# Optimization experiments

Hardware: AMD Instinct MI355X
Metric: run time of the kernel (lower is better)

Reference implementation:

```python
import jax, jax.numpy as jnp
import numpy as np

B, K, S, H, V, T = 32, 5, 64, 768, 30522, 40
SEP = 102


def setup_inputs() -> dict:
    key = jax.random.key(0)
    ks = jax.random.split(key, 8)
    s = 0.02
    return {
        "src": jax.random.normal(ks[0], (B, S, H), jnp.float32),
        "E": jax.random.normal(ks[1], (V, H), jnp.float32) * s,
        "Wa": jax.random.normal(ks[2], (H, H), jnp.float32) * s,
        "Ua": jax.random.normal(ks[3], (H, H), jnp.float32) * s,
        "va": jax.random.normal(ks[4], (H,), jnp.float32) * s,
        "W_ih": jax.random.normal(ks[5], (3 * H, 2 * H), jnp.float32) * s,
        "W_hh": jax.random.normal(ks[6], (3 * H, H), jnp.float32) * s,
        "b_ih": jnp.zeros((3 * H,), jnp.float32),
        "b_hh": jnp.zeros((3 * H,), jnp.float32),
        "Wo": jax.random.normal(ks[7], (V, H), jnp.float32) * s,
        "bo": jnp.zeros((V,), jnp.float32),
    }


def _decoder(tok, src, h, E, Wa, Ua, va, W_ih, W_hh, b_ih, b_hh, Wo, bo):
    # tok [N] int, src [N,S,H], h [N,H] -> (logits [N,V], h_new [N,H])
    emb = E[tok]                                              # [N,H]
    e = jnp.tanh(src @ Wa + (h @ Ua)[:, None, :]) @ va        # [N,S]
    a = jax.nn.softmax(e, axis=-1)
    ctx = jnp.einsum('ns,nsd->nd', a, src)                    # [N,H]
    x = jnp.concatenate([emb, ctx], axis=-1)                  # [N,2H]
    gx = x @ W_ih.T + b_ih
    gh = h @ W_hh.T + b_hh
    xr, xz, xn = jnp.split(gx, 3, axis=-1)
    hr, hz, hn = jnp.split(gh, 3, axis=-1)
    r = jax.nn.sigmoid(xr + hr)
    z = jax.nn.sigmoid(xz + hz)
    n = jnp.tanh(xn + r * hn)
    h2 = (1.0 - z) * n + z * h
    return h2 @ Wo.T + bo, h2


def _search(src, E, Wa, Ua, va, W_ih, W_hh, b_ih, b_hh, Wo, bo):
    P = (E, Wa, Ua, va, W_ih, W_hh, b_ih, b_hh, Wo, bo)
    # step 0: start token 102, zero hidden
    tok0 = jnp.full((B,), SEP, jnp.int32)
    logits, h = _decoder(tok0, src, jnp.zeros((B, H), src.dtype), *P)
    logp = jax.nn.log_softmax(logits, axis=-1)
    scores, toks = jax.lax.top_k(logp, K)                     # [B,K]
    hiddens = jnp.broadcast_to(h[:, None, :], (B, K, H))
    src_k = jnp.broadcast_to(src[:, None], (B, K, S, H)).reshape(B * K, S, H)
    no_prob = jnp.full((V,), -1e9, src.dtype).at[SEP].set(0.0)
    beam_mask = jnp.arange(K) < K - 1  # original normalizes only first k-1 segments

    def body(carry, _):
        toks, maps, hiddens, scores, ended, lengths = carry
        # parent hidden per beam (gather by backpointer), decode all beams at once
        h_in = jnp.take_along_axis(hiddens, maps[:, :, None], axis=1)  # [B,K,H]
        logits, h_new = _decoder(toks.reshape(-1), src_k, h_in.reshape(B * K, H), *P)
        logp = jax.nn.log_softmax(logits, axis=-1).reshape(B, K, V)
        logp = jnp.where(ended[:, :, None] == 0, logp, no_prob)
        lengths = lengths + (ended == 0).astype(lengths.dtype)
        cand = logp + scores[:, :, None]                      # [B,K,V]
        denom = jnp.where(beam_mask, lengths ** 0.7, 1.0)     # [B,K]
        norm = (cand / denom[:, :, None]).reshape(B, K * V)
        _, idx = jax.lax.top_k(norm, K)                       # [B,K]
        new_scores = jnp.take_along_axis(cand.reshape(B, K * V), idx, axis=1)
        new_toks = (idx % V).astype(jnp.int32)
        new_maps = (idx // V).astype(jnp.int32)
        ended = jnp.where(new_toks == SEP, 1.0, ended)
        new_carry = (new_toks, new_maps, h_new.reshape(B, K, H), new_scores, ended, lengths)
        return new_carry, (new_toks, new_maps)

    carry0 = (toks.astype(jnp.int32), jnp.zeros((B, K), jnp.int32), hiddens,
              scores, jnp.zeros((B, K), src.dtype), jnp.zeros((B, K), src.dtype))
    carryF, (toks_seq, maps_seq) = jax.lax.scan(body, carry0, None, length=T - 1)
    toks_all = jnp.concatenate([toks[None].astype(jnp.int32), toks_seq], axis=0)   # [T,B,K]
    maps_all = jnp.concatenate([jnp.zeros((1, B, K), jnp.int32), maps_seq], axis=0)
    final_scores = carryF[3]
    best = jnp.argmax(final_scores, axis=1).astype(jnp.int32)  # [B]

    def back(idx, tm):
        tk, mp = tm
        out = jnp.take_along_axis(tk, idx[:, None], axis=1)[:, 0]
        nxt = jnp.take_along_axis(mp, idx[:, None], axis=1)[:, 0]
        return nxt, out

    _, outs = jax.lax.scan(back, best, (toks_all, maps_all), reverse=True)
    return outs.T, final_scores  # tokens [B,T], scores [B,K]


def reference(src, E, Wa, Ua, va, W_ih, W_hh, b_ih, b_hh, Wo, bo):
    tokens, _ = _search(src, E, Wa, Ua, va, W_ih, W_hh, b_ih, b_hh, Wo, bo)
    return tokens
```

## Files before the change

kernel.cpp:

```cpp
#include <hip/hip_runtime.h>
#include <hip/hip_cooperative_groups.h>
#include <cmath>

namespace cg = cooperative_groups;

#define Hdim 768
#define Bb 32
#define Kb 5
#define Ss 64
#define Vv 30522
#define Tt 40
#define SEPTOK 102
#define NTLOG 477

typedef __attribute__((ext_vector_type(2))) float f32x2;
typedef __attribute__((ext_vector_type(4))) float f32x4;

struct Params {
    const float *src, *E, *Wa, *Ua, *va, *W_ih, *W_hh, *b_ih, *b_hh, *Wo, *bo;
    float *srcWa, *hA, *hB, *h_tmp, *h_g, *hUa, *xbuf, *gxE, *gx, *gh, *logits;
    float *mt_g; double *st_g; float *t5v; int *t5j;
    float *mx, *lgs, *scores, *ended, *lengths;
    int *toks_cur, *maps_cur, *toks_all, *maps_all, *outTok;
};

__device__ __forceinline__ bool betterf(float va, int ja, float vb, int jb) {
    return (va > vb) || (va == vb && ja < jb);
}
__device__ __forceinline__ void ins5(float* tv, int* tj, float v, int j) {
    if (!betterf(v, j, tv[4], tj[4])) return;
    tv[4] = v; tj[4] = j;
#pragma unroll
    for (int q = 4; q > 0; q--) {
        if (betterf(tv[q], tj[q], tv[q - 1], tj[q - 1])) {
            float t = tv[q]; tv[q] = tv[q - 1]; tv[q - 1] = t;
            int  ti = tj[q]; tj[q] = tj[q - 1]; tj[q - 1] = ti;
        }
    }
}
__device__ __forceinline__ void ins5p(float* tv, int* tj, float* tx,
                                      float v, int j, float x) {
    if (!betterf(v, j, tv[4], tj[4])) return;
    tv[4] = v; tj[4] = j; tx[4] = x;
#pragma unroll
    for (int q = 4; q > 0; q--) {
        if (betterf(tv[q], tj[q], tv[q - 1], tj[q - 1])) {
            float t = tv[q]; tv[q] = tv[q - 1]; tv[q - 1] = t;
            int  ti = tj[q]; tj[q] = tj[q - 1]; tj[q - 1] = ti;
            float tz = tx[q]; tx[q] = tx[q - 1]; tx[q - 1] = tz;
        }
    }
}

union SMem {
    struct { float xs[32][162]; float wt[32][68]; } g;
    struct { float hu[Hdim]; float va[Hdim]; float e[Ss]; float a[Ss];
             float ctx[Hdim]; float gx[2304]; } at;
    struct { float sc[Kb], den[Kb], end[Kb], len[Kb], mxs[Kb], lgv[Kb];
             float mv[256 * 5]; int mj[256 * 5]; float mxp[256 * 5];
             float rv[512]; int rj[512]; float rx[512]; double rd[512];
             int selj[Kb]; float selx[Kb]; } tk;
};

__device__ void gemm512(SMem& sm, const Params& P, int t, int N, int xsrc,
    int i0, int Pdim, const float* __restrict__ W, int ldW, bool pmaj,
    const float* __restrict__ bias, float* __restrict__ outp, int ldO, int Icap)
{
    const int tid = threadIdx.x;
    const int ty = tid >> 5, tx = tid & 31;
    const float* h_old = (t & 1) ? P.hB : P.hA;

    float acc[10][2];
#pragma unroll
    for (int j = 0; j < 10; j++) { acc[j][0] = 0.f; acc[j][1] = 0.f; }

    for (int c0 = 0; c0 < Pdim; c0 += 32) {
        __syncthreads();
        for (int e = tid; e < 160 * 32; e += 512) {
            int r = e >> 5, p = e & 31;
            int n = (r < N) ? r : (N - 1);
            float v = 0.f;
            if (xsrc == 0) {
                if (t != 0) {
                    int par = (n / Kb) * Kb + P.maps_cur[n];
                    v = h_old[(size_t)par * Hdim + c0 + p];
                }
            } else {
                int tok = (t == 0) ? SEPTOK : P.toks_cur[n];
                v = P.E[(size_t)tok * Hdim + c0 + p];
            }
            sm.g.xs[p][r] = v;
        }
        if (pmaj) {
            int p = tid >> 4, i4 = (tid & 15) * 4;
            int gi = i0 + i4;
            f32x4 a;
            if (gi + 3 < Icap) {
                a = *(const f32x4*)&W[(size_t)(c0 + p) * ldW + gi];
            } else {
#pragma unroll
                for (int u = 0; u < 4; u++) {
                    int g = gi + u; if (g >= Icap) g = Icap - 1;
                    a[u] = W[(size_t)(c0 + p) * ldW + g];
                }
            }
            *(f32x4*)&sm.g.wt[p][i4] = a;
        } else {
            int c = tid >> 3, p4 = (tid & 7) * 4;
            int gi = i0 + c; if (gi >= Icap) gi = Icap - 1;
            f32x4 a = *(const f32x4*)&W[(size_t)gi * ldW + c0 + p4];
            sm.g.wt[p4 + 0][c] = a[0]; sm.g.wt[p4 + 1][c] = a[1];
            sm.g.wt[p4 + 2][c] = a[2]; sm.g.wt[p4 + 3][c] = a[3];
        }
        __syncthreads();
        float part[10][2];
#pragma unroll
        for (int j = 0; j < 10; j++) { part[j][0] = 0.f; part[j][1] = 0.f; }
#pragma unroll
        for (int p = 0; p < 32; p++) {
            f32x2 w2 = *(const f32x2*)&sm.g.wt[p][tx * 2];
            float xr[10];
#pragma unroll
            for (int j = 0; j < 10; j += 2) {
                f32x2 xv = *(const f32x2*)&sm.g.xs[p][ty * 10 + j];
                xr[j] = xv.x; xr[j + 1] = xv.y;
            }
#pragma unroll
            for (int j = 0; j < 10; j++) {
                part[j][0] = fmaf(xr[j], w2.x, part[j][0]);
                part[j][1] = fmaf(xr[j], w2.y, part[j][1]);
            }
        }
#pragma unroll
        for (int j = 0; j < 10; j++) {
            acc[j][0] = __fadd_rn(acc[j][0], part[j][0]);
            acc[j][1] = __fadd_rn(acc[j][1], part[j][1]);
        }
    }
#pragma unroll
    for (int j = 0; j < 10; j++) {
        int r = ty * 10 + j;
        if (r < N) {
#pragma unroll
            for (int u = 0; u < 2; u++) {
                int gi = i0 + tx * 2 + u;
                if (gi < Icap) {
                    float v = acc[j][u];
                    if (bias) v = __fadd_rn(v, bias[gi]);
                    outp[(size_t)r * ldO + gi] = v;
                }
            }
        }
    }
}

__device__ void logits_tile(SMem& sm, const Params& P, int t, int N, int task)
{
    const int tid = threadIdx.x;
    const int ty = tid >> 5, tx = tid & 31;
    const int i0 = task * 64;
    const float* h_new = (t & 1) ? P.hA : P.hB;
    const int rowMul = (t == 0) ? Kb : 1;

    float acc[10][2];
#pragma unroll
    for (int j = 0; j < 10; j++) { acc[j][0] = 0.f; acc[j][1] = 0.f; }

    for (int c0 = 0; c0 < Hdim; c0 += 32) {
        __syncthreads();
        for (int e = tid; e < 160 * 32; e += 512) {
            int r = e >> 5, p = e & 31;
            int n = (r < N) ? r : (N - 1);
            sm.g.xs[p][r] = h_new[((size_t)n * rowMul) * Hdim + c0 + p];
        }
        {
            int c = tid >> 3, p4 = (tid & 7) * 4;
            int gi = i0 + c; if (gi >= Vv) gi = Vv - 1;
            f32x4 a = *(const f32x4*)&P.Wo[(size_t)gi * Hdim + c0 + p4];
            sm.g.wt[p4 + 0][c] = a[0]; sm.g.wt[p4 + 1][c] = a[1];
            sm.g.wt[p4 + 2][c] = a[2]; sm.g.wt[p4 + 3][c] = a[3];
        }
        __syncthreads();
        float part[10][2];
#pragma unroll
        for (int j = 0; j < 10; j++) { part[j][0] = 0.f; part[j][1] = 0.f; }
#pragma unroll
        for (int p = 0; p < 32; p++) {
            f32x2 w2 = *(const f32x2*)&sm.g.wt[p][tx * 2];
            float xr[10];
#pragma unroll
            for (int j = 0; j < 10; j += 2) {
                f32x2 xv = *(const f32x2*)&sm.g.xs[p][ty * 10 + j];
                xr[j] = xv.x; xr[j + 1] = xv.y;
            }
#pragma unroll
            for (int j = 0; j < 10; j++) {
                part[j][0] = fmaf(xr[j], w2.x, part[j][0]);
                part[j][1] = fmaf(xr[j], w2.y, part[j][1]);
            }
        }
#pragma unroll
        for (int j = 0; j < 10; j++) {
            acc[j][0] = __fadd_rn(acc[j][0], part[j][0]);
            acc[j][1] = __fadd_rn(acc[j][1], part[j][1]);
        }
    }
#pragma unroll
    for (int j = 0; j < 10; j++) {
        int r = ty * 10 + j;
        int g0 = i0 + tx * 2, g1 = g0 + 1;
        float x0 = (g0 < Vv) ? __fadd_rn(acc[j][0], P.bo[g0]) : -INFINITY;
        float x1 = (g1 < Vv) ? __fadd_rn(acc[j][1], P.bo[g1]) : -INFINITY;
        float mr = fmaxf(x0, x1);
#pragma unroll
        for (int off = 16; off; off >>= 1)
            mr = fmaxf(mr, __shfl_xor(mr, off, 32));
        double s = (double)expf(__fsub_rn(x0, mr)) + (double)expf(__fsub_rn(x1, mr));
#pragma unroll
        for (int off = 16; off; off >>= 1)
            s += __shfl_xor(s, off, 32);
        float tv[5]; int tj[5];
#pragma unroll
        for (int q = 0; q < 5; q++) { tv[q] = -INFINITY; tj[q] = 0x7fffffff; }
        ins5(tv, tj, x0, (g0 < Vv) ? g0 : 0x7fffffff);
        ins5(tv, tj, x1, (g1 < Vv) ? g1 : 0x7fffffff);
#pragma unroll
        for (int lv = 1; lv < 32; lv <<= 1) {
            float pv[5]; int pj[5];
#pragma unroll
            for (int q = 0; q < 5; q++) {
                pv[q] = __shfl_xor(tv[q], lv, 32);
                pj[q] = __shfl_xor(tj[q], lv, 32);
            }
#pragma unroll
            for (int q = 0; q < 5; q++) ins5(tv, tj, pv[q], pj[q]);
        }
        if (tx == 0 && r < N) {
            P.mt_g[(size_t)task * 160 + r] = mr;
            P.st_g[(size_t)task * 160 + r] = s;
#pragma unroll
            for (int q = 0; q < 5; q++) {
                P.t5v[((size_t)task * 160 + r) * 5 + q] = tv[q];
                P.t5j[((size_t)task * 160 + r) * 5 + q] = tj[q];
            }
        }
    }
}

__global__ __launch_bounds__(512) void step_k(Params P)
{
    cg::grid_group grid = cg::this_grid();
    __shared__ SMem sm;
    const int tid = threadIdx.x;
    const int gdim = gridDim.x;

    for (int t = 0; t < Tt; t++) {
        const int N = (t == 0) ? Bb : Bb * Kb;
        const int Kcur = (t == 0) ? 1 : Kb;
        float* h_new = (t & 1) ? P.hA : P.hB;
        const float* h_old = (t & 1) ? P.hB : P.hA;

        for (int task = blockIdx.x; task < 84; task += gdim) {
            if (task < 12)
                gemm512(sm, P, t, N, 0, task * 64, Hdim, P.Ua, Hdim, true,
                        nullptr, P.hUa, Hdim, Hdim);
            else if (task < 48)
                gemm512(sm, P, t, N, 0, (task - 12) * 64, Hdim, P.W_hh, Hdim, false,
                        P.b_hh, P.gh, 2304, 2304);
            else
                gemm512(sm, P, t, N, 1, (task - 48) * 64, Hdim, P.W_ih, 1536, false,
                        nullptr, P.gxE, 2304, 2304);
        }
        grid.sync();

        for (int n = blockIdx.x; n < N; n += gdim) {
            int b = n / Kcur;
            for (int j = tid; j < Hdim; j += 512) {
                sm.at.hu[j] = P.hUa[(size_t)n * Hdim + j];
                sm.at.va[j] = P.va[j];
            }
            __syncthreads();
            {
                int wv = tid >> 6, ln = tid & 63;
                for (int s = wv * 8; s < wv * 8 + 8; s++) {
                    const float* sw = P.srcWa + (size_t)(b * Ss + s) * Hdim;
                    double p = 0.0;
                    for (int j = ln; j < Hdim; j += 64) {
                        float tv = tanhf(__fadd_rn(sw[j], sm.at.hu[j]));
                        p = ::fma((double)tv, (double)sm.at.va[j], p);
                    }
                    for (int off = 32; off; off >>= 1) p += __shfl_down(p, off, 64);
                    if (ln == 0) sm.at.e[s] = (float)p;
                }
            }
            __syncthreads();
            if (tid < 64) {
                float v = sm.at.e[tid], m = v;
                for (int off = 32; off; off >>= 1) m = fmaxf(m, __shfl_xor(m, off, 64));
                float p = expf(__fsub_rn(v, m));
                double sum = (double)p;
                for (int off = 32; off; off >>= 1) sum += __shfl_xor(sum, off, 64);
                sm.at.a[tid] = __fdiv_rn(p, (float)sum);
            }
            __syncthreads();
            for (int j = tid; j < Hdim; j += 512) {
                double acc = 0.0;
                for (int s = 0; s < Ss; s++)
                    acc = ::fma((double)sm.at.a[s],
                                (double)P.src[(size_t)(b * Ss + s) * Hdim + j], acc);
                sm.at.ctx[j] = (float)acc;
            }
            __syncthreads();
            for (int i = tid; i < 2304; i += 512) {
                const float* wr = P.W_ih + (size_t)i * 1536 + 768;
                float accv = 0.f, part = 0.f;
                for (int p = 0; p < 768; p += 4) {
                    f32x4 w4 = *(const f32x4*)&wr[p];
                    part = fmaf(sm.at.ctx[p + 0], w4[0], part);
                    part = fmaf(sm.at.ctx[p + 1], w4[1], part);
                    part = fmaf(sm.at.ctx[p + 2], w4[2], part);
                    part = fmaf(sm.at.ctx[p + 3], w4[3], part);
                    if ((p & 31) == 28) { accv = __fadd_rn(accv, part); part = 0.f; }
                }
                sm.at.gx[i] = __fadd_rn(__fadd_rn(P.gxE[(size_t)n * 2304 + i], accv),
                                        P.b_ih[i]);
            }
            __syncthreads();
            int par = 0;
            if (t != 0) par = (n / Kb) * Kb + P.maps_cur[n];
            for (int i = tid; i < Hdim; i += 512) {
                float xr = sm.at.gx[i], xz = sm.at.gx[768 + i], xn = sm.at.gx[1536 + i];
                const float* ghr = P.gh + (size_t)n * 2304;
                float hr = ghr[i], hz = ghr[768 + i], hn = ghr[1536 + i];
                float r  = __fdiv_rn(1.f, __fadd_rn(1.f, expf(-__fadd_rn(xr, hr))));
                float z  = __fdiv_rn(1.f, __fadd_rn(1.f, expf(-__fadd_rn(xz, hz))));
                float nn = tanhf(__fadd_rn(xn, __fmul_rn(r, hn)));
                float hv = (t == 0) ? 0.f : h_old[(size_t)par * Hdim + i];
                float h2 = __fadd_rn(__fmul_rn(__fsub_rn(1.f, z), nn), __fmul_rn(z, hv));
                if (t == 0) {
                    for (int k = 0; k < Kb; k++)
                        h_new[(size_t)(n * Kb + k) * Hdim + i] = h2;
                } else {
                    h_new[(size_t)n * Hdim + i] = h2;
                }
            }
            __syncthreads();
        }
        grid.sync();

        for (int task = blockIdx.x; task < NTLOG; task += gdim)
            logits_tile(sm, P, t, N, task);
        grid.sync();

        for (int b = blockIdx.x; b < Bb; b += gdim) {
            if (tid < Kb) {
                if (t == 0) {
                    sm.tk.sc[tid] = 0.f; sm.tk.end[tid] = 0.f; sm.tk.len[tid] = 0.f;
                    sm.tk.den[tid] = 1.f;
                } else {
                    float e0 = P.ended[b * Kb + tid];
                    float ln = __fadd_rn(P.lengths[b * Kb + tid], (e0 == 0.f) ? 1.f : 0.f);
                    sm.tk.sc[tid]  = P.scores[b * Kb + tid];
                    sm.tk.end[tid] = e0;
                    sm.tk.len[tid] = ln;
                    sm.tk.den[tid] = (tid < Kb - 1) ? (float)pow((double)ln, (double)0.7f) : 1.f;
                }
            }
            __syncthreads();
            for (int k = 0; k < Kcur; k++) {
                bool active = (t == 0) || (sm.tk.end[k] == 0.f);
                if (!active) {
                    if (tid == 0) { sm.tk.mxs[k] = 0.f; sm.tk.lgv[k] = 0.f; }
                    __syncthreads();
                    continue;
                }
                int n = b * Kcur + k;
                float m = -INFINITY;
                for (int tile = tid; tile < NTLOG; tile += 512)
                    m = fmaxf(m, P.mt_g[(size_t)tile * 160 + n]);
                sm.tk.rv[tid] = m; __syncthreads();
                for (int off = 256; off; off >>= 1) {
                    if (tid < off) sm.tk.rv[tid] = fmaxf(sm.tk.rv[tid], sm.tk.rv[tid + off]);
                    __syncthreads();
                }
                m = sm.tk.rv[0];
                double s = 0.0;
                for (int tile = tid; tile < NTLOG; tile += 512)
                    s += P.st_g[(size_t)tile * 160 + n] *
                         exp((double)(P.mt_g[(size_t)tile * 160 + n] - m));
                __syncthreads();
                sm.tk.rd[tid] = s; __syncthreads();
                for (int off = 256; off; off >>= 1) {
                    if (tid < off) sm.tk.rd[tid] += sm.tk.rd[tid + off];
                    __syncthreads();
                }
                if (tid == 0) {
                    sm.tk.mxs[k] = m;
                    float sf = (float)sm.tk.rd[0];
                    sm.tk.lgv[k] = (float)log((double)sf);
                }
                __syncthreads();
            }
            float tv[5]; int tj[5]; float txx[5];
#pragma unroll
            for (int q = 0; q < 5; q++) { tv[q] = -INFINITY; tj[q] = 0x7fffffff; txx[q] = 0.f; }
            if (tid < 256) {
                int tot = Kcur * NTLOG * 5;
                for (int c = tid; c < tot; c += 256) {
                    int k = c / (NTLOG * 5);
                    if (t != 0 && sm.tk.end[k] != 0.f) continue;
                    int rm = c - k * NTLOG * 5;
                    int tile = rm / 5, q = rm - tile * 5;
                    int n = b * Kcur + k;
                    int gi = P.t5j[((size_t)tile * 160 + n) * 5 + q];
                    if (gi == 0x7fffffff) continue;
                    float x = P.t5v[((size_t)tile * 160 + n) * 5 + q];
                    float lp  = __fsub_rn(__fsub_rn(x, sm.tk.mxs[k]), sm.tk.lgv[k]);
                    float val = __fdiv_rn(__fadd_rn(lp, sm.tk.sc[k]), sm.tk.den[k]);
                    ins5p(tv, tj, txx, val, k * Vv + gi, x);
                }
            }
            if (tid == 0 && t != 0) {
                for (int k = 0; k < Kcur; k++)
                    if (sm.tk.end[k] != 0.f) {
                        float val = __fdiv_rn(sm.tk.sc[k], sm.tk.den[k]);
                        ins5p(tv, tj, txx, val, k * Vv + SEPTOK, 0.f);
                    }
            }
            if (tid < 256) {
#pragma unroll
                for (int q = 0; q < 5; q++) {
                    sm.tk.mv[tid * 5 + q] = tv[q];
                    sm.tk.mj[tid * 5 + q] = tj[q];
                    sm.tk.mxp[tid * 5 + q] = txx[q];
                }
            }
            __syncthreads();
            for (int pass = 0; pass < Kb; pass++) {
                if (tid < 256) {
                    float bv = -INFINITY; int bj = 0x7fffffff; float bx = 0.f;
#pragma unroll
                    for (int q = 0; q < 5; q++) {
                        float v = sm.tk.mv[tid * 5 + q]; int j = sm.tk.mj[tid * 5 + q];
                        if (betterf(v, j, bv, bj)) { bv = v; bj = j; bx = sm.tk.mxp[tid * 5 + q]; }
                    }
                    sm.tk.rv[tid] = bv; sm.tk.rj[tid] = bj; sm.tk.rx[tid] = bx;
                }
                __syncthreads();
                for (int off = 128; off; off >>= 1) {
                    if (tid < off) {
                        float ov = sm.tk.rv[tid + off]; int oj = sm.tk.rj[tid + off];
                        if (betterf(ov, oj, sm.tk.rv[tid], sm.tk.rj[tid])) {
                            sm.tk.rv[tid] = ov; sm.tk.rj[tid] = oj;
                            sm.tk.rx[tid] = sm.tk.rx[tid + off];
                        }
                    }
                    __syncthreads();
                }
                if (tid == 0) { sm.tk.selj[pass] = sm.tk.rj[0]; sm.tk.selx[pass] = sm.tk.rx[0]; }
                __syncthreads();
                if (tid < 256) {
#pragma unroll
                    for (int q = 0; q < 5; q++)
                        if (sm.tk.mj[tid * 5 + q] == sm.tk.selj[pass]) {
                            sm.tk.mv[tid * 5 + q] = -INFINITY;
                            sm.tk.mj[tid * 5 + q] = 0x7fffffff;
                        }
                }
                __syncthreads();
            }
            if (tid == 0) {
                for (int q = 0; q < Kb; q++) {
                    int jj = sm.tk.selj[q];
                    int pk = jj / Vv, vv = jj - pk * Vv;
                    float lp;
                    if (t == 0 || sm.tk.end[pk] == 0.f)
                        lp = __fsub_rn(__fsub_rn(sm.tk.selx[q], sm.tk.mxs[pk]), sm.tk.lgv[pk]);
                    else
                        lp = (vv == SEPTOK) ? 0.f : -1e9f;
                    float cand = __fadd_rn(lp, sm.tk.sc[pk]);
                    P.scores[b * Kb + q]   = cand;
                    P.toks_cur[b * Kb + q] = vv;
                    P.maps_cur[b * Kb + q] = (t == 0) ? 0 : pk;
                    if (t == 0) {
                        P.ended[b * Kb + q]   = 0.f;
                        P.lengths[b * Kb + q] = 0.f;
                    } else {
                        P.ended[b * Kb + q]   = (vv == SEPTOK) ? 1.f : sm.tk.end[q];
                        P.lengths[b * Kb + q] = sm.tk.len[q];
                    }
                    P.toks_all[(size_t)t * Bb * Kb + b * Kb + q] = vv;
                    P.maps_all[(size_t)t * Bb * Kb + b * Kb + q] = (t == 0) ? 0 : pk;
                }
            }
            __syncthreads();
        }
        grid.sync();
    }

    if (blockIdx.x == 0 && tid < Bb) {
        int b = tid;
        int best = 0; float bvv = P.scores[b * Kb];
        for (int k = 1; k < Kb; k++) {
            float v = P.scores[b * Kb + k];
            if (v > bvv) { bvv = v; best = k; }
        }
        int cur = best;
        for (int t = Tt - 1; t >= 0; t--) {
            P.outTok[b * Tt + t] = P.toks_all[t * Bb * Kb + b * Kb + cur];
            cur = P.maps_all[t * Bb * Kb + b * Kb + cur];
        }
    }
}

template<int RPT, int CPT, bool PMAJ>
__global__ __launch_bounds__(512) void gemmN_k(int P, int I, int xrs, int ldW,
    const float* __restrict__ X, const float* __restrict__ W,
    const float* __restrict__ bias, float* __restrict__ out, int ldO)
{
    constexpr int ROWS = RPT * 16;
    constexpr int COLS = CPT * 32;
    constexpr int XST  = ROWS + 4;
    constexpr int WST  = COLS + 4;
    __shared__ float xs[32][XST];
    __shared__ float wt[32][WST];
    const int tid = threadIdx.x;
    const int ty = tid >> 5, tx = tid & 31;
    const int row0 = blockIdx.y * ROWS;
    const int i0 = blockIdx.x * COLS;

    float acc[RPT][CPT];
#pragma unroll
    for (int j = 0; j < RPT; j++)
#pragma unroll
        for (int u = 0; u < CPT; u++) acc[j][u] = 0.f;

    for (int c0 = 0; c0 < P; c0 += 32) {
        __syncthreads();
        for (int e = tid; e < ROWS * 32; e += 512) {
            int r = e >> 5, p = e & 31;
            xs[p][r] = X[(size_t)(row0 + r) * xrs + c0 + p];
        }
        if (PMAJ) {
            for (int v = tid; v < 32 * (COLS / 4); v += 512) {
                int p  = v / (COLS / 4);
                int i4 = (v % (COLS / 4)) * 4;
                f32x4 a;
                if (i0 + i4 + 3 < I) {
                    a = *(const f32x4*)&W[(size_t)(c0 + p) * ldW + i0 + i4];
                } else {
#pragma unroll
                    for (int u = 0; u < 4; u++) {
                        int g = i0 + i4 + u; if (g >= I) g = I - 1;
                        a[u] = W[(size_t)(c0 + p) * ldW + g];
                    }
                }
                *(f32x4*)&wt[p][i4] = a;
            }
        } else {
            for (int v = tid; v < COLS * 8; v += 512) {
                int c  = v >> 3;
                int p4 = (v & 7) * 4;
                int gi = i0 + c; if (gi >= I) gi = I - 1;
                f32x4 a = *(const f32x4*)&W[(size_t)gi * ldW + c0 + p4];
                wt[p4 + 0][c] = a[0]; wt[p4 + 1][c] = a[1];
                wt[p4 + 2][c] = a[2]; wt[p4 + 3][c] = a[3];
            }
        }
        __syncthreads();
        float part[RPT][CPT];
#pragma unroll
        for (int j = 0; j < RPT; j++)
#pragma unroll
            for (int u = 0; u < CPT; u++) part[j][u] = 0.f;
#pragma unroll
        for (int p = 0; p < 32; p++) {
            float xr[RPT];
#pragma unroll
            for (int j = 0; j < RPT; j += 2) {
                f32x2 xv = *(const f32x2*)&xs[p][ty * RPT + j];
                xr[j] = xv.x; xr[j + 1] = xv.y;
            }
            float wv[CPT];
#pragma unroll
            for (int u = 0; u < CPT; u += 2) {
                f32x2 w2 = *(const f32x2*)&wt[p][tx * CPT + u];
                wv[u] = w2.x; wv[u + 1] = w2.y;
            }
#pragma unroll
            for (int j = 0; j < RPT; j++)
#pragma unroll
                for (int u = 0; u < CPT; u++)
                    part[j][u] = fmaf(xr[j], wv[u], part[j][u]);
        }
#pragma unroll
        for (int j = 0; j < RPT; j++)
#pragma unroll
            for (int u = 0; u < CPT; u++)
                acc[j][u] = __fadd_rn(acc[j][u], part[j][u]);
    }
#pragma unroll
    for (int j = 0; j < RPT; j++) {
        int gr = row0 + ty * RPT + j;
#pragma unroll
        for (int u = 0; u < CPT; u++) {
            int gi = i0 + tx * CPT + u;
            if (gi < I) {
                float v = acc[j][u];
                if (bias) v = __fadd_rn(v, bias[gi]);
                out[(size_t)gr * ldO + gi] = v;
            }
        }
    }
}

__global__ __launch_bounds__(256) void gather_k(int N, int Kcur,
    const int* __restrict__ maps, const int* __restrict__ toks,
    const float* __restrict__ h_beam, const float* __restrict__ E,
    float* __restrict__ h_g, float* __restrict__ xbuf)
{
    int n = blockIdx.x;
    if (n >= N) return;
    int b = n / Kcur;
    int tok = toks ? toks[n] : SEPTOK;
    const float* er = E + (size_t)tok * Hdim;
    if (maps) {
        const float* hs = h_beam + (size_t)(b * Kb + maps[n]) * Hdim;
        for (int j = threadIdx.x; j < Hdim; j += 256) {
            h_g[(size_t)n * Hdim + j]  = hs[j];
            xbuf[(size_t)n * 1536 + j] = er[j];
        }
    } else {
        for (int j = threadIdx.x; j < Hdim; j += 256) {
            h_g[(size_t)n * Hdim + j]  = 0.f;
            xbuf[(size_t)n * 1536 + j] = er[j];
        }
    }
}

__global__ __launch_bounds__(256) void bcast_k(const float* __restrict__ h_tmp,
                                               float* __restrict__ h_beam)
{
    int b = blockIdx.x;
    for (int j = threadIdx.x; j < Hdim; j += 256) {
        float v = h_tmp[(size_t)b * Hdim + j];
        for (int k = 0; k < Kb; k++)
            h_beam[(size_t)(b * Kb + k) * Hdim + j] = v;
    }
}

__global__ __launch_bounds__(256) void attn2_k(int N, int Kcur,
    const float* __restrict__ hUa, const float* __restrict__ srcWa,
    const float* __restrict__ src, const float* __restrict__ va,
    float* __restrict__ xbuf)
{
    __shared__ float hu[Hdim];
    __shared__ float va_s[Hdim];
    __shared__ float e_s[Ss];
    __shared__ float a_s[Ss];
    int n = blockIdx.x, tid = threadIdx.x;
    if (n >= N) return;
    int b = n / Kcur;
    for (int j = tid; j < Hdim; j += 256) {
        hu[j]   = hUa[(size_t)n * Hdim + j];
        va_s[j] = va[j];
    }
    __syncthreads();
    int wv = tid >> 6, ln = tid & 63;
    for (int s = wv * 16; s < wv * 16 + 16; s++) {
        const float* sw = srcWa + (size_t)(b * Ss + s) * Hdim;
        double p = 0.0;
        for (int j = ln; j < Hdim; j += 64) {
            float tv = (float)tanh((double)__fadd_rn(sw[j], hu[j]));
            p = ::fma((double)tv, (double)va_s[j], p);
        }
        for (int off = 32; off; off >>= 1) p += __shfl_down(p, off, 64);
        if (ln == 0) e_s[s] = (float)p;
    }
    __syncthreads();
    if (tid < 64) {
        float v = e_s[tid], m = v;
        for (int off = 32; off; off >>= 1) m = fmaxf(m, __shfl_xor(m, off, 64));
        float p = (float)exp((double)__fsub_rn(v, m));
        double sum = (double)p;
        for (int off = 32; off; off >>= 1) sum += __shfl_xor(sum, off, 64);
        a_s[tid] = __fdiv_rn(p, (float)sum);
    }
    __syncthreads();
    for (int j = tid; j < Hdim; j += 256) {
        double acc = 0.0;
        for (int s = 0; s < Ss; s++)
            acc = ::fma((double)a_s[s], (double)src[(size_t)(b * Ss + s) * Hdim + j], acc);
        xbuf[(size_t)n * 1536 + 768 + j] = (float)acc;
    }
}

__global__ __launch_bounds__(256) void gate_k(int N,
    const float* __restrict__ gx, const float* __restrict__ gh,
    const float* __restrict__ h_g, float* __restrict__ h_out)
{
    int idx = blockIdx.x * 256 + threadIdx.x;
    if (idx >= N * Hdim) return;
    int n = idx / Hdim, i = idx - n * Hdim;
    const float* gxr = gx + (size_t)n * 2304;
    const float* ghr = gh + (size_t)n * 2304;
    float xr = gxr[i], xz = gxr[768 + i], xn = gxr[1536 + i];
    float hr = ghr[i], hz = ghr[768 + i], hn = ghr[1536 + i];
    float r  = (float)(1.0 / (1.0 + exp(-(double)__fadd_rn(xr, hr))));
    float z  = (float)(1.0 / (1.0 + exp(-(double)__fadd_rn(xz, hz))));
    float nn = (float)tanh((double)__fadd_rn(xn, __fmul_rn(r, hn)));
    float hv = h_g[(size_t)n * Hdim + i];
    float h2 = __fadd_rn(__fmul_rn(__fsub_rn(1.f, z), nn), __fmul_rn(z, hv));
    h_out[(size_t)n * Hdim + i] = h2;
}

__global__ __launch_bounds__(256) void lse_k(int N,
    const float* __restrict__ logits, float* __restrict__ mx, float* __restrict__ lgs)
{
    __shared__ float  redf[256];
    __shared__ double redd[256];
    int n = blockIdx.x, tid = threadIdx.x;
    const float* lg = logits + (size_t)n * Vv;
    float m = -INFINITY;
    for (int v = tid; v < Vv; v += 256) m = fmaxf(m, lg[v]);
    redf[tid] = m; __syncthreads();
    for (int off = 128; off; off >>= 1) {
        if (tid < off) redf[tid] = fmaxf(redf[tid], redf[tid + off]);
        __syncthreads();
    }
    m = redf[0];
    double s = 0.0;
    for (int v = tid; v < Vv; v += 256) {
        float ex = (float)exp((double)__fsub_rn(lg[v], m));
        s += (double)ex;
    }
    redd[tid] = s; __syncthreads();
    for (int off = 128; off; off >>= 1) {
        if (tid < off) redd[tid] += redd[tid + off];
        __syncthreads();
    }
    if (tid == 0) {
        mx[n] = m;
        float sf = (float)redd[0];
        lgs[n] = (float)log((double)sf);
    }
}

__global__ __launch_bounds__(256) void topk5_k(int t,
    const float* __restrict__ logits, const float* __restrict__ mx, const float* __restrict__ lgs,
    float* scores, float* ended, float* lengths,
    int* toks_cur, int* maps_cur, int* toks_all, int* maps_all)
{
    __shared__ float sc_s[Kb], den_s[Kb], end_s[Kb], len_s[Kb], mx_s[Kb], lg_s[Kb];
    __shared__ float mv[256 * 5];
    __shared__ int   mj[256 * 5];
    __shared__ float rv[256];
    __shared__ int   rj[256];
    __shared__ int   selj[Kb];
    int b = blockIdx.x, tid = threadIdx.x;
    int Kcur = (t == 0) ? 1 : Kb;
    if (tid < Kb) {
        if (t == 0) {
            sc_s[tid] = 0.f; end_s[tid] = 0.f; len_s[tid] = 0.f; den_s[tid] = 1.f;
            mx_s[tid] = mx[b]; lg_s[tid] = lgs[b];
        } else {
            float e0 = ended[b * Kb + tid];
            float ln = __fadd_rn(lengths[b * Kb + tid], (e0 == 0.f) ? 1.f : 0.f);
            sc_s[tid]  = scores[b * Kb + tid];
            end_s[tid] = e0;
            len_s[tid] = ln;
            den_s[tid] = (tid < Kb - 1) ? (float)pow((double)ln, (double)0.7f) : 1.f;
            mx_s[tid]  = mx[b * Kb + tid];
            lg_s[tid]  = lgs[b * Kb + tid];
        }
    }
    __syncthreads();
    const float* lbase = logits + (size_t)b * Kcur * Vv;
    float tv[5]; int tj[5];
#pragma unroll
    for (int q = 0; q < 5; q++) { tv[q] = -INFINITY; tj[q] = 0x7fffffff; }
    for (int k = 0; k < Kcur; k++) {
        if (end_s[k] == 0.f) {
            float m = mx_s[k], l = lg_s[k], sck = sc_s[k], den = den_s[k];
            const float* lg = lbase + (size_t)k * Vv;
            for (int v = tid; v < Vv; v += 256) {
                float lp  = __fsub_rn(__fsub_rn(lg[v], m), l);
                float val = __fdiv_rn(__fadd_rn(lp, sck), den);
                ins5(tv, tj, val, k * Vv + v);
            }
        } else if (tid == 0) {
            float val = __fdiv_rn(sc_s[k], den_s[k]);
            ins5(tv, tj, val, k * Vv + SEPTOK);
        }
    }
#pragma unroll
    for (int q = 0; q < 5; q++) { mv[tid * 5 + q] = tv[q]; mj[tid * 5 + q] = tj[q]; }
    __syncthreads();
    for (int pass = 0; pass < Kb; pass++) {
        float bv = -INFINITY; int bj = 0x7fffffff;
#pragma unroll
        for (int q = 0; q < 5; q++) {
            float v = mv[tid * 5 + q]; int j = mj[tid * 5 + q];
            if (betterf(v, j, bv, bj)) { bv = v; bj = j; }
        }
        rv[tid] = bv; rj[tid] = bj;
        __syncthreads();
        for (int off = 128; off; off >>= 1) {
            if (tid < off) {
                float ov = rv[tid + off]; int oj = rj[tid + off];
                if (betterf(ov, oj, rv[tid], rj[tid])) { rv[tid] = ov; rj[tid] = oj; }
            }
            __syncthreads();
        }
        if (tid == 0) selj[pass] = rj[0];
        __syncthreads();
#pragma unroll
        for (int q = 0; q < 5; q++)
            if (mj[tid * 5 + q] == selj[pass]) { mv[tid * 5 + q] = -INFINITY; mj[tid * 5 + q] = 0x7fffffff; }
        __syncthreads();
    }
    if (tid == 0) {
        for (int q = 0; q < Kb; q++) {
            int jj = selj[q];
            int pk = jj / Vv, vv = jj - pk * Vv;
            float lp;
            if (end_s[pk] == 0.f)
                lp = __fsub_rn(__fsub_rn(lbase[(size_t)pk * Vv + vv], mx_s[pk]), lg_s[pk]);
            else
                lp = (vv == SEPTOK) ? 0.f : -1e9f;
            float cand = __fadd_rn(lp, sc_s[pk]);
            scores[b * Kb + q]   = cand;
            toks_cur[b * Kb + q] = vv;
            maps_cur[b * Kb + q] = (t == 0) ? 0 : pk;
            if (t == 0) {
                ended[b * Kb + q]   = 0.f;
                lengths[b * Kb + q] = 0.f;
            } else {
                ended[b * Kb + q]   = (vv == SEPTOK) ? 1.f : end_s[q];
                lengths[b * Kb + q] = len_s[q];
            }
            toks_all[(size_t)t * Bb * Kb + b * Kb + q] = vv;
            maps_all[(size_t)t * Bb * Kb + b * Kb + q] = (t == 0) ? 0 : pk;
        }
    }
}

__global__ void back_k(const float* __restrict__ scores,
                       const int* __restrict__ toks_all, const int* __restrict__ maps_all,
                       int* __restrict__ out)
{
    int b = threadIdx.x;
    if (b >= Bb) return;
    int best = 0; float bvv = scores[b * Kb];
    for (int k = 1; k < Kb; k++) {
        float v = scores[b * Kb + k];
        if (v > bvv) { bvv = v; best = k; }
    }
    int cur = best;
    for (int t = Tt - 1; t >= 0; t--) {
        out[b * Tt + t] = toks_all[t * Bb * Kb + b * Kb + cur];
        cur = maps_all[t * Bb * Kb + b * Kb + cur];
    }
}

extern "C" void kernel_launch(void* const* d_in, const int* in_sizes, int n_in,
                              void* d_out, int out_size, void* d_ws, size_t ws_size,
                              hipStream_t stream)
{
    Params P;
    P.src  = (const float*)d_in[0];
    P.E    = (const float*)d_in[1];
    P.Wa   = (const float*)d_in[2];
    P.Ua   = (const float*)d_in[3];
    P.va   = (const float*)d_in[4];
    P.W_ih = (const float*)d_in[5];
    P.W_hh = (const float*)d_in[6];
    P.b_ih = (const float*)d_in[7];
    P.b_hh = (const float*)d_in[8];
    P.Wo   = (const float*)d_in[9];
    P.bo   = (const float*)d_in[10];
    P.outTok = (int*)d_out;

    char* w = (char*)d_ws;
    size_t used = 0;
    auto alloc = [&](size_t bytes) -> char* {
        char* p = w + used;
        used += (bytes + 255) & ~(size_t)255;
        return p;
    };
    P.srcWa   = (float*)alloc((size_t)Bb * Ss * Hdim * 4);
    P.hA      = (float*)alloc((size_t)Bb * Kb * Hdim * 4);
    P.hB      = (float*)alloc((size_t)Bb * Kb * Hdim * 4);
    P.h_tmp   = (float*)alloc((size_t)Bb * Hdim * 4);
    P.h_g     = (float*)alloc((size_t)Bb * Kb * Hdim * 4);
    P.hUa     = (float*)alloc((size_t)Bb * Kb * Hdim * 4);
    P.xbuf    = (float*)alloc((size_t)Bb * Kb * 1536 * 4);
    P.gxE     = (float*)alloc((size_t)Bb * Kb * 2304 * 4);
    P.gx      = (float*)alloc((size_t)Bb * Kb * 2304 * 4);
    P.gh      = (float*)alloc((size_t)Bb * Kb * 2304 * 4);
    P.logits  = (float*)alloc((size_t)Bb * Kb * Vv * 4);
    P.mt_g    = (float*)alloc((size_t)NTLOG * 160 * 4);
    P.st_g    = (double*)alloc((size_t)NTLOG * 160 * 8);
    P.t5v     = (float*)alloc((size_t)NTLOG * 160 * 5 * 4);
    P.t5j     = (int*)alloc((size_t)NTLOG * 160 * 5 * 4);
    P.mx      = (float*)alloc(Bb * Kb * 4);
    P.lgs     = (float*)alloc(Bb * Kb * 4);
    P.scores  = (float*)alloc(Bb * Kb * 4);
    P.ended   = (float*)alloc(Bb * Kb * 4);
    P.lengths = (float*)alloc(Bb * Kb * 4);
    P.toks_cur = (int*)alloc(Bb * Kb * 4);
    P.maps_cur = (int*)alloc(Bb * Kb * 4);
    P.toks_all = (int*)alloc((size_t)Tt * Bb * Kb * 4);
    P.maps_all = (int*)alloc((size_t)Tt * Bb * Kb * 4);

    gemmN_k<8, 2, true><<<dim3(12, 16), 512, 0, stream>>>(
        Hdim, Hdim, Hdim, Hdim, P.src, P.Wa, nullptr, P.srcWa, Hdim);

    int dev = 0;
    (void)hipGetDevice(&dev);
    int nCU = 256;
    (void)hipDeviceGetAttribute(&nCU, hipDeviceAttributeMultiprocessorCount, dev);
    int maxAct = 0;
    if (hipOccupancyMaxActiveBlocksPerMultiprocessor(&maxAct, step_k, 512, 0)
            != hipSuccess || maxAct < 1)
        maxAct = 1;
    long long gridLL = (long long)maxAct * (long long)nCU;
    if (gridLL > 512) gridLL = 512;
    if (gridLL < 1) gridLL = 1;
    dim3 grid((unsigned)gridLL);

    void* args[] = { (void*)&P };
    hipError_t err = hipLaunchCooperativeKernel((void*)step_k, grid, dim3(512),
                                                args, 0, stream);
    if (err != hipSuccess) {
        (void)hipGetLastError();
        for (int t = 0; t < Tt; t++) {
            int N  = (t == 0) ? Bb : Bb * Kb;
            int Kc = (t == 0) ? 1 : Kb;
            const int* mp = (t == 0) ? nullptr : P.maps_cur;
            const int* tk = (t == 0) ? nullptr : P.toks_cur;
            float* h_beam = P.hA;
            float* h_cur = (t == 0) ? P.h_tmp : h_beam;

            gather_k<<<N, 256, 0, stream>>>(N, Kc, mp, tk, h_beam, P.E, P.h_g, P.xbuf);
            if (t == 0) {
                gemmN_k<2, 2, true><<<dim3(12, 1), 512, 0, stream>>>(
                    Hdim, Hdim, Hdim, Hdim, P.h_g, P.Ua, nullptr, P.hUa, Hdim);
            } else {
                gemmN_k<10, 2, true><<<dim3(12, 1), 512, 0, stream>>>(
                    Hdim, Hdim, Hdim, Hdim, P.h_g, P.Ua, nullptr, P.hUa, Hdim);
            }
            attn2_k<<<N, 256, 0, stream>>>(N, Kc, P.hUa, P.srcWa, P.src, P.va, P.xbuf);
            if (t == 0) {
                gemmN_k<2, 2, false><<<dim3(36, 1), 512, 0, stream>>>(
                    1536, 2304, 1536, 1536, P.xbuf, P.W_ih, P.b_ih, P.gx, 2304);
                gemmN_k<2, 2, false><<<dim3(36, 1), 512, 0, stream>>>(
                    Hdim, 2304, Hdim, Hdim, P.h_g, P.W_hh, P.b_hh, P.gh, 2304);
            } else {
                gemmN_k<10, 2, false><<<dim3(36, 1), 512, 0, stream>>>(
                    1536, 2304, 1536, 1536, P.xbuf, P.W_ih, P.b_ih, P.gx, 2304);
                gemmN_k<10, 2, false><<<dim3(36, 1), 512, 0, stream>>>(
                    Hdim, 2304, Hdim, Hdim, P.h_g, P.W_hh, P.b_hh, P.gh, 2304);
            }
            gate_k<<<(N * Hdim + 255) / 256, 256, 0, stream>>>(N, P.gx, P.gh, P.h_g, h_cur);
            if (t == 0)
                bcast_k<<<Bb, 256, 0, stream>>>(P.h_tmp, h_beam);
            if (t == 0) {
                gemmN_k<2, 4, false><<<dim3(239, 1), 512, 0, stream>>>(
                    Hdim, Vv, Hdim, Hdim, h_cur, P.Wo, P.bo, P.logits, Vv);
            } else {
                gemmN_k<10, 4, false><<<dim3(239, 1), 512, 0, stream>>>(
                    Hdim, Vv, Hdim, Hdim, h_cur, P.Wo, P.bo, P.logits, Vv);
            }
            lse_k<<<N, 256, 0, stream>>>(N, P.logits, P.mx, P.lgs);
            topk5_k<<<Bb, 256, 0, stream>>>(t, P.logits, P.mx, P.lgs, P.scores,
                                            P.ended, P.lengths, P.toks_cur, P.maps_cur,
                                            P.toks_all, P.maps_all);
        }
        back_k<<<1, 64, 0, stream>>>(P.scores, P.toks_all, P.maps_all, P.outTok);
    }
}
```

Before: 47.31 ms.

## Replace cooperative persistent kernel with per-phase kernel launches

Splits the single cooperative grid-synchronized step kernel into four separate kernels per decode step (projection GEMMs, attention plus GRU, logits tiles, top-k), launched in a host loop, and drops the old multi-kernel fallback path. Grid-wide barriers become kernel boundaries, and each phase gets its own grid size and smaller shared memory footprint, which may raise occupancy. The cost is about 160 kernel launches with their launch gaps, in exchange for removing grid.sync overhead and the occupancy limit set by the largest shared-memory union.

```diff
diff --git a/kernel.cpp b/kernel.cpp
--- a/kernel.cpp
+++ b/kernel.cpp
@@ -1,8 +1,5 @@
 #include <hip/hip_runtime.h>
-#include <hip/hip_cooperative_groups.h>
 #include <cmath>
-
-namespace cg = cooperative_groups;
 
 #define Hdim 768
 #define Bb 32
@@ -18,9 +15,9 @@
 
 struct Params {
     const float *src, *E, *Wa, *Ua, *va, *W_ih, *W_hh, *b_ih, *b_hh, *Wo, *bo;
-    float *srcWa, *hA, *hB, *h_tmp, *h_g, *hUa, *xbuf, *gxE, *gx, *gh, *logits;
+    float *srcWa, *hA, *hB, *hUa, *gxE, *gh;
     float *mt_g; double *st_g; float *t5v; int *t5j;
-    float *mx, *lgs, *scores, *ended, *lengths;
+    float *scores, *ended, *lengths;
     int *toks_cur, *maps_cur, *toks_all, *maps_all, *outTok;
 };
 
@@ -52,17 +49,9 @@
     }
 }
 
-union SMem {
-    struct { float xs[32][162]; float wt[32][68]; } g;
-    struct { float hu[Hdim]; float va[Hdim]; float e[Ss]; float a[Ss];
-             float ctx[Hdim]; float gx[2304]; } at;
-    struct { float sc[Kb], den[Kb], end[Kb], len[Kb], mxs[Kb], lgv[Kb];
-             float mv[256 * 5]; int mj[256 * 5]; float mxp[256 * 5];
-             float rv[512]; int rj[512]; float rx[512]; double rd[512];
-             int selj[Kb]; float selx[Kb]; } tk;
-};
-
-__device__ void gemm512(SMem& sm, const Params& P, int t, int N, int xsrc,
+struct GS { float xs[32][162]; float wt[32][68]; };
+
+__device__ void gemm512(GS& sm, const Params& P, int t, int N, int xsrc,
     int i0, int Pdim, const float* __restrict__ W, int ldW, bool pmaj,
     const float* __restrict__ bias, float* __restrict__ outp, int ldO, int Icap)
 {
@@ -89,7 +78,7 @@
                 int tok = (t == 0) ? SEPTOK : P.toks_cur[n];
                 v = P.E[(size_t)tok * Hdim + c0 + p];
             }
-            sm.g.xs[p][r] = v;
+            sm.xs[p][r] = v;
         }
         if (pmaj) {
             int p = tid >> 4, i4 = (tid & 15) * 4;
@@ -104,13 +93,13 @@
                     a[u] = W[(size_t)(c0 + p) * ldW + g];
                 }
             }
-            *(f32x4*)&sm.g.wt[p][i4] = a;
+            *(f32x4*)&sm.wt[p][i4] = a;
         } else {
             int c = tid >> 3, p4 = (tid & 7) * 4;
             int gi = i0 + c; if (gi >= Icap) gi = Icap - 1;
             f32x4 a = *(const f32x4*)&W[(size_t)gi * ldW + c0 + p4];
-            sm.g.wt[p4 + 0][c] = a[0]; sm.g.wt[p4 + 1][c] = a[1];
-            sm.g.wt[p4 + 2][c] = a[2]; sm.g.wt[p4 + 3][c] = a[3];
+            sm.wt[p4 + 0][c] = a[0]; sm.wt[p4 + 1][c] = a[1];
+            sm.wt[p4 + 2][c] = a[2]; sm.wt[p4 + 3][c] = a[3];
         }
         __syncthreads();
         float part[10][2];
@@ -118,11 +107,11 @@
         for (int j = 0; j < 10; j++) { part[j][0] = 0.f; part[j][1] = 0.f; }
 #pragma unroll
         for (int p = 0; p < 32; p++) {
-            f32x2 w2 = *(const f32x2*)&sm.g.wt[p][tx * 2];
+            f32x2 w2 = *(const f32x2*)&sm.wt[p][tx * 2];
             float xr[10];
 #pragma unroll
             for (int j = 0; j < 10; j += 2) {
-                f32x2 xv = *(const f32x2*)&sm.g.xs[p][ty * 10 + j];
+                f32x2 xv = *(const f32x2*)&sm.xs[p][ty * 10 + j];
                 xr[j] = xv.x; xr[j + 1] = xv.y;
             }
 #pragma unroll
@@ -154,10 +143,113 @@
     }
 }
 
-__device__ void logits_tile(SMem& sm, const Params& P, int t, int N, int task)
-{
+__global__ __launch_bounds__(512) void p1_k(Params P, int t, int N)
+{
+    __shared__ GS sm;
+    int task = blockIdx.x;
+    if (task < 12)
+        gemm512(sm, P, t, N, 0, task * 64, Hdim, P.Ua, Hdim, true,
+                nullptr, P.hUa, Hdim, Hdim);
+    else if (task < 48)
+        gemm512(sm, P, t, N, 0, (task - 12) * 64, Hdim, P.W_hh, Hdim, false,
+                P.b_hh, P.gh, 2304, 2304);
+    else
+        gemm512(sm, P, t, N, 1, (task - 48) * 64, Hdim, P.W_ih, 1536, false,
+                nullptr, P.gxE, 2304, 2304);
+}
+
+__global__ __launch_bounds__(512) void p2_k(Params P, int t, int N)
+{
+    __shared__ float hu[Hdim];
+    __shared__ float va_s[Hdim];
+    __shared__ float e_s[Ss];
+    __shared__ float a_s[Ss];
+    __shared__ float ctx[Hdim];
+    __shared__ float gx[2304];
+    const int tid = threadIdx.x;
+    const int n = blockIdx.x;
+    if (n >= N) return;
+    const int Kcur = (t == 0) ? 1 : Kb;
+    const int b = n / Kcur;
+    float* h_new = (t & 1) ? P.hA : P.hB;
+    const float* h_old = (t & 1) ? P.hB : P.hA;
+
+    for (int j = tid; j < Hdim; j += 512) {
+        hu[j]   = P.hUa[(size_t)n * Hdim + j];
+        va_s[j] = P.va[j];
+    }
+    __syncthreads();
+    {
+        int wv = tid >> 6, ln = tid & 63;
+        for (int s = wv * 8; s < wv * 8 + 8; s++) {
+            const float* sw = P.srcWa + (size_t)(b * Ss + s) * Hdim;
+            double p = 0.0;
+            for (int j = ln; j < Hdim; j += 64) {
+                float tv = tanhf(__fadd_rn(sw[j], hu[j]));
+                p = ::fma((double)tv, (double)va_s[j], p);
+            }
+            for (int off = 32; off; off >>= 1) p += __shfl_down(p, off, 64);
+            if (ln == 0) e_s[s] = (float)p;
+        }
+    }
+    __syncthreads();
+    if (tid < 64) {
+        float v = e_s[tid], m = v;
+        for (int off = 32; off; off >>= 1) m = fmaxf(m, __shfl_xor(m, off, 64));
+        float p = expf(__fsub_rn(v, m));
+        double sum = (double)p;
+        for (int off = 32; off; off >>= 1) sum += __shfl_xor(sum, off, 64);
+        a_s[tid] = __fdiv_rn(p, (float)sum);
+    }
+    __syncthreads();
+    for (int j = tid; j < Hdim; j += 512) {
+        double acc = 0.0;
+        for (int s = 0; s < Ss; s++)
+            acc = ::fma((double)a_s[s],
+                        (double)P.src[(size_t)(b * Ss + s) * Hdim + j], acc);
+        ctx[j] = (float)acc;
+    }
+    __syncthreads();
+    for (int i = tid; i < 2304; i += 512) {
+        const float* wr = P.W_ih + (size_t)i * 1536 + 768;
+        float accv = 0.f, part = 0.f;
+        for (int p = 0; p < 768; p += 4) {
+            f32x4 w4 = *(const f32x4*)&wr[p];
+            part = fmaf(ctx[p + 0], w4[0], part);
+            part = fmaf(ctx[p + 1], w4[1], part);
+            part = fmaf(ctx[p + 2], w4[2], part);
+            part = fmaf(ctx[p + 3], w4[3], part);
+            if ((p & 31) == 28) { accv = __fadd_rn(accv, part); part = 0.f; }
+        }
+        gx[i] = __fadd_rn(__fadd_rn(P.gxE[(size_t)n * 2304 + i], accv), P.b_ih[i]);
+    }
+    __syncthreads();
+    int par = 0;
+    if (t != 0) par = (n / Kb) * Kb + P.maps_cur[n];
+    for (int i = tid; i < Hdim; i += 512) {
+        float xr = gx[i], xz = gx[768 + i], xn = gx[1536 + i];
+        const float* ghr = P.gh + (size_t)n * 2304;
+        float hr = ghr[i], hz = ghr[768 + i], hn = ghr[1536 + i];
+        float r  = __fdiv_rn(1.f, __fadd_rn(1.f, expf(-__fadd_rn(xr, hr))));
+        float z  = __fdiv_rn(1.f, __fadd_rn(1.f, expf(-__fadd_rn(xz, hz))));
+        float nn = tanhf(__fadd_rn(xn, __fmul_rn(r, hn)));
+        float hv = (t == 0) ? 0.f : h_old[(size_t)par * Hdim + i];
+        float h2 = __fadd_rn(__fmul_rn(__fsub_rn(1.f, z), nn), __fmul_rn(z, hv));
+        if (t == 0) {
+            for (int k = 0; k < Kb; k++)
+                h_new[(size_t)(n * Kb + k) * Hdim + i] = h2;
+        } else {
+            h_new[(size_t)n * Hdim + i] = h2;
+        }
+    }
+}
+
+__global__ __launch_bounds__(512) void p4_k(Params P, int t, int N)
+{
+    __shared__ GS sm;
     const int tid = threadIdx.x;
     const int ty = tid >> 5, tx = tid & 31;
+    const int task = blockIdx.x;
     const int i0 = task * 64;
     const float* h_new = (t & 1) ? P.hA : P.hB;
     const int rowMul = (t == 0) ? Kb : 1;
@@ -171,14 +263,14 @@
         for (int e = tid; e < 160 * 32; e += 512) {
             int r = e >> 5, p = e & 31;
             int n = (r < N) ? r : (N - 1);
-            sm.g.xs[p][r] = h_new[((size_t)n * rowMul) * Hdim + c0 + p];
+            sm.xs[p][r] = h_new[((size_t)n * rowMul) * Hdim + c0 + p];
         }
         {
             int c = tid >> 3, p4 = (tid & 7) * 4;
             int gi = i0 + c; if (gi >= Vv) gi = Vv - 1;
             f32x4 a = *(const f32x4*)&P.Wo[(size_t)gi * Hdim + c0 + p4];
-            sm.g.wt[p4 + 0][c] = a[0]; sm.g.wt[p4 + 1][c] = a[1];
-            sm.g.wt[p4 + 2][c] = a[2]; sm.g.wt[p4 + 3][c] = a[3];
+            sm.wt[p4 + 0][c] = a[0]; sm.wt[p4 + 1][c] = a[1];
+            sm.wt[p4 + 2][c] = a[2]; sm.wt[p4 + 3][c] = a[3];
         }
         __syncthreads();
         float part[10][2];
@@ -186,11 +278,11 @@
         for (int j = 0; j < 10; j++) { part[j][0] = 0.f; part[j][1] = 0.f; }
 #pragma unroll
         for (int p = 0; p < 32; p++) {
-            f32x2 w2 = *(const f32x2*)&sm.g.wt[p][tx * 2];
+            f32x2 w2 = *(const f32x2*)&sm.wt[p][tx * 2];
             float xr[10];
 #pragma unroll
             for (int j = 0; j < 10; j += 2) {
-                f32x2 xv = *(const f32x2*)&sm.g.xs[p][ty * 10 + j];
+                f32x2 xv = *(const f32x2*)&sm.xs[p][ty * 10 + j];
                 xr[j] = xv.x; xr[j + 1] = xv.y;
             }
 #pragma unroll
@@ -247,269 +339,171 @@
     }
 }
 
-__global__ __launch_bounds__(512) void step_k(Params P)
-{
-    cg::grid_group grid = cg::this_grid();
-    __shared__ SMem sm;
+__global__ __launch_bounds__(512) void p5_k(Params P, int t)
+{
+    __shared__ float sc[Kb], den[Kb], endd[Kb], len[Kb], mxs[Kb], lgv[Kb];
+    __shared__ float mv[256 * 5]; __shared__ int mj[256 * 5];
+    __shared__ float mxp[256 * 5];
+    __shared__ float rv[512]; __shared__ int rj[512]; __shared__ float rx[512];
+    __shared__ double rd[512];
+    __shared__ int selj[Kb]; __shared__ float selx[Kb];
     const int tid = threadIdx.x;
-    const int gdim = gridDim.x;
-
-    for (int t = 0; t < Tt; t++) {
-        const int N = (t == 0) ? Bb : Bb * Kb;
-        const int Kcur = (t == 0) ? 1 : Kb;
-        float* h_new = (t & 1) ? P.hA : P.hB;
-        const float* h_old = (t & 1) ? P.hB : P.hA;
-
-        for (int task = blockIdx.x; task < 84; task += gdim) {
-            if (task < 12)
-                gemm512(sm, P, t, N, 0, task * 64, Hdim, P.Ua, Hdim, true,
-                        nullptr, P.hUa, Hdim, Hdim);
-            else if (task < 48)
-                gemm512(sm, P, t, N, 0, (task - 12) * 64, Hdim, P.W_hh, Hdim, false,
-                        P.b_hh, P.gh, 2304, 2304);
+    const int b = blockIdx.x;
+    const int Kcur = (t == 0) ? 1 : Kb;
+
+    if (tid < Kb) {
+        if (t == 0) {
+            sc[tid] = 0.f; endd[tid] = 0.f; len[tid] = 0.f; den[tid] = 1.f;
+        } else {
+            float e0 = P.ended[b * Kb + tid];
+            float ln = __fadd_rn(P.lengths[b * Kb + tid], (e0 == 0.f) ? 1.f : 0.f);
+            sc[tid]  = P.scores[b * Kb + tid];
+            endd[tid] = e0;
+            len[tid] = ln;
+            den[tid] = (tid < Kb - 1) ? (float)pow((double)ln, (double)0.7f) : 1.f;
+        }
+    }
+    __syncthreads();
+    for (int k = 0; k < Kcur; k++) {
+        bool active = (t == 0) || (endd[k] == 0.f);
+        if (!active) {
+            if (tid == 0) { mxs[k] = 0.f; lgv[k] = 0.f; }
+            __syncthreads();
+            continue;
+        }
+        int n = b * Kcur + k;
+        float m = -INFINITY;
+        for (int tile = tid; tile < NTLOG; tile += 512)
+            m = fmaxf(m, P.mt_g[(size_t)tile * 160 + n]);
+        rv[tid] = m; __syncthreads();
+        for (int off = 256; off; off >>= 1) {
+            if (tid < off) rv[tid] = fmaxf(rv[tid], rv[tid + off]);
+            __syncthreads();
+        }
+        m = rv[0];
+        double s = 0.0;
+        for (int tile = tid; tile < NTLOG; tile += 512)
+            s += P.st_g[(size_t)tile * 160 + n] *
+                 exp((double)(P.mt_g[(size_t)tile * 160 + n] - m));
+        __syncthreads();
+        rd[tid] = s; __syncthreads();
+        for (int off = 256; off; off >>= 1) {
+            if (tid < off) rd[tid] += rd[tid + off];
+            __syncthreads();
+        }
+        if (tid == 0) {
+            mxs[k] = m;
+            float sf = (float)rd[0];
+            lgv[k] = (float)log((double)sf);
+        }
+        __syncthreads();
+    }
+    float tv[5]; int tj[5]; float txx[5];
+#pragma unroll
+    for (int q = 0; q < 5; q++) { tv[q] = -INFINITY; tj[q] = 0x7fffffff; txx[q] = 0.f; }
+    if (tid < 256) {
+        int tot = Kcur * NTLOG * 5;
+        for (int c = tid; c < tot; c += 256) {
+            int k = c / (NTLOG * 5);
+            if (t != 0 && endd[k] != 0.f) continue;
+            int rm = c - k * NTLOG * 5;
+            int tile = rm / 5, q = rm - tile * 5;
+            int n = b * Kcur + k;
+            int gi = P.t5j[((size_t)tile * 160 + n) * 5 + q];
+            if (gi == 0x7fffffff) continue;
+            float x = P.t5v[((size_t)tile * 160 + n) * 5 + q];
+            float lp  = __fsub_rn(__fsub_rn(x, mxs[k]), lgv[k]);
+            float val = __fdiv_rn(__fadd_rn(lp, sc[k]), den[k]);
+            ins5p(tv, tj, txx, val, k * Vv + gi, x);
+        }
+    }
+    if (tid == 0 && t != 0) {
+        for (int k = 0; k < Kcur; k++)
+            if (endd[k] != 0.f) {
+                float val = __fdiv_rn(sc[k], den[k]);
+                ins5p(tv, tj, txx, val, k * Vv + SEPTOK, 0.f);
+            }
+    }
+    if (tid < 256) {
+#pragma unroll
+        for (int q = 0; q < 5; q++) {
+            mv[tid * 5 + q] = tv[q];
+            mj[tid * 5 + q] = tj[q];
+            mxp[tid * 5 + q] = txx[q];
+        }
+    }
+    __syncthreads();
+    for (int pass = 0; pass < Kb; pass++) {
+        if (tid < 256) {
+            float bv = -INFINITY; int bj = 0x7fffffff; float bx = 0.f;
+#pragma unroll
+            for (int q = 0; q < 5; q++) {
+                float v = mv[tid * 5 + q]; int j = mj[tid * 5 + q];
+                if (betterf(v, j, bv, bj)) { bv = v; bj = j; bx = mxp[tid * 5 + q]; }
+            }
+            rv[tid] = bv; rj[tid] = bj; rx[tid] = bx;
+        }
+        __syncthreads();
+        for (int off = 128; off; off >>= 1) {
+            if (tid < off) {
+                float ov = rv[tid + off]; int oj = rj[tid + off];
+                if (betterf(ov, oj, rv[tid], rj[tid])) {
+                    rv[tid] = ov; rj[tid] = oj; rx[tid] = rx[tid + off];
+                }
+            }
+            __syncthreads();
+        }
+        if (tid == 0) { selj[pass] = rj[0]; selx[pass] = rx[0]; }
+        __syncthreads();
+        if (tid < 256) {
+#pragma unroll
+            for (int q = 0; q < 5; q++)
+                if (mj[tid * 5 + q] == selj[pass]) {
+                    mv[tid * 5 + q] = -INFINITY;
+                    mj[tid * 5 + q] = 0x7fffffff;
+                }
+        }
+        __syncthreads();
+    }
+    if (tid == 0) {
+        for (int q = 0; q < Kb; q++) {
+            int jj = selj[q];
+            int pk = jj / Vv, vv = jj - pk * Vv;
+            float lp;
+            if (t == 0 || endd[pk] == 0.f)
+                lp = __fsub_rn(__fsub_rn(selx[q], mxs[pk]), lgv[pk]);
             else
-                gemm512(sm, P, t, N, 1, (task - 48) * 64, Hdim, P.W_ih, 1536, false,
-                        nullptr, P.gxE, 2304, 2304);
-        }
-        grid.sync();
-
-        for (int n = blockIdx.x; n < N; n += gdim) {
-            int b = n / Kcur;
-            for (int j = tid; j < Hdim; j += 512) {
-                sm.at.hu[j] = P.hUa[(size_t)n * Hdim + j];
-                sm.at.va[j] = P.va[j];
-            }
-            __syncthreads();
-            {
-                int wv = tid >> 6, ln = tid & 63;
-                for (int s = wv * 8; s < wv * 8 + 8; s++) {
-                    const float* sw = P.srcWa + (size_t)(b * Ss + s) * Hdim;
-                    double p = 0.0;
-                    for (int j = ln; j < Hdim; j += 64) {
-                        float tv = tanhf(__fadd_rn(sw[j], sm.at.hu[j]));
-                        p = ::fma((double)tv, (double)sm.at.va[j], p);
-                    }
-                    for (int off = 32; off; off >>= 1) p += __shfl_down(p, off, 64);
-                    if (ln == 0) sm.at.e[s] = (float)p;
-                }
-            }
-            __syncthreads();
-            if (tid < 64) {
-                float v = sm.at.e[tid], m = v;
-                for (int off = 32; off; off >>= 1) m = fmaxf(m, __shfl_xor(m, off, 64));
-                float p = expf(__fsub_rn(v, m));
-                double sum = (double)p;
-                for (int off = 32; off; off >>= 1) sum += __shfl_xor(sum, off, 64);
-                sm.at.a[tid] = __fdiv_rn(p, (float)sum);
-            }
-            __syncthreads();
-            for (int j = tid; j < Hdim; j += 512) {
-                double acc = 0.0;
-                for (int s = 0; s < Ss; s++)
-                    acc = ::fma((double)sm.at.a[s],
-                                (double)P.src[(size_t)(b * Ss + s) * Hdim + j], acc);
-                sm.at.ctx[j] = (float)acc;
-            }
-            __syncthreads();
-            for (int i = tid; i < 2304; i += 512) {
-                const float* wr = P.W_ih + (size_t)i * 1536 + 768;
-                float accv = 0.f, part = 0.f;
-                for (int p = 0; p < 768; p += 4) {
-                    f32x4 w4 = *(const f32x4*)&wr[p];
-                    part = fmaf(sm.at.ctx[p + 0], w4[0], part);
-                    part = fmaf(sm.at.ctx[p + 1], w4[1], part);
-                    part = fmaf(sm.at.ctx[p + 2], w4[2], part);
-                    part = fmaf(sm.at.ctx[p + 3], w4[3], part);
-                    if ((p & 31) == 28) { accv = __fadd_rn(accv, part); part = 0.f; }
-                }
-                sm.at.gx[i] = __fadd_rn(__fadd_rn(P.gxE[(size_t)n * 2304 + i], accv),
-                                        P.b_ih[i]);
-            }
-            __syncthreads();
-            int par = 0;
-            if (t != 0) par = (n / Kb) * Kb + P.maps_cur[n];
-            for (int i = tid; i < Hdim; i += 512) {
-                float xr = sm.at.gx[i], xz = sm.at.gx[768 + i], xn = sm.at.gx[1536 + i];
-                const float* ghr = P.gh + (size_t)n * 2304;
-                float hr = ghr[i], hz = ghr[768 + i], hn = ghr[1536 + i];
-                float r  = __fdiv_rn(1.f, __fadd_rn(1.f, expf(-__fadd_rn(xr, hr))));
-                float z  = __fdiv_rn(1.f, __fadd_rn(1.f, expf(-__fadd_rn(xz, hz))));
-                float nn = tanhf(__fadd_rn(xn, __fmul_rn(r, hn)));
-                float hv = (t == 0) ? 0.f : h_old[(size_t)par * Hdim + i];
-                float h2 = __fadd_rn(__fmul_rn(__fsub_rn(1.f, z), nn), __fmul_rn(z, hv));
-                if (t == 0) {
-                    for (int k = 0; k < Kb; k++)
-                        h_new[(size_t)(n * Kb + k) * Hdim + i] = h2;
-                } else {
-                    h_new[(size_t)n * Hdim + i] = h2;
-                }
-            }
-            __syncthreads();
-        }
-        grid.sync();
-
-        for (int task = blockIdx.x; task < NTLOG; task += gdim)
-            logits_tile(sm, P, t, N, task);
-        grid.sync();
-
-        for (int b = blockIdx.x; b < Bb; b += gdim) {
-            if (tid < Kb) {
-                if (t == 0) {
-                    sm.tk.sc[tid] = 0.f; sm.tk.end[tid] = 0.f; sm.tk.len[tid] = 0.f;
-                    sm.tk.den[tid] = 1.f;
-                } else {
-                    float e0 = P.ended[b * Kb + tid];
-                    float ln = __fadd_rn(P.lengths[b * Kb + tid], (e0 == 0.f) ? 1.f : 0.f);
-                    sm.tk.sc[tid]  = P.scores[b * Kb + tid];
-                    sm.tk.end[tid] = e0;
-                    sm.tk.len[tid] = ln;
-                    sm.tk.den[tid] = (tid < Kb - 1) ? (float)pow((double)ln, (double)0.7f) : 1.f;
-                }
-            }
-            __syncthreads();
-            for (int k = 0; k < Kcur; k++) {
-                bool active = (t == 0) || (sm.tk.end[k] == 0.f);
-                if (!active) {
-                    if (tid == 0) { sm.tk.mxs[k] = 0.f; sm.tk.lgv[k] = 0.f; }
-                    __syncthreads();
-                    continue;
-                }
-                int n = b * Kcur + k;
-                float m = -INFINITY;
-                for (int tile = tid; tile < NTLOG; tile += 512)
-                    m = fmaxf(m, P.mt_g[(size_t)tile * 160 + n]);
-                sm.tk.rv[tid] = m; __syncthreads();
-                for (int off = 256; off; off >>= 1) {
-                    if (tid < off) sm.tk.rv[tid] = fmaxf(sm.tk.rv[tid], sm.tk.rv[tid + off]);
-                    __syncthreads();
-                }
-                m = sm.tk.rv[0];
-                double s = 0.0;
-                for (int tile = tid; tile < NTLOG; tile += 512)
-                    s += P.st_g[(size_t)tile * 160 + n] *
-                         exp((double)(P.mt_g[(size_t)tile * 160 + n] - m));
-                __syncthreads();
-                sm.tk.rd[tid] = s; __syncthreads();
-                for (int off = 256; off; off >>= 1) {
-                    if (tid < off) sm.tk.rd[tid] += sm.tk.rd[tid + off];
-                    __syncthreads();
-                }
-                if (tid == 0) {
-                    sm.tk.mxs[k] = m;
-                    float sf = (float)sm.tk.rd[0];
-                    sm.tk.lgv[k] = (float)log((double)sf);
-                }
-                __syncthreads();
-            }
-            float tv[5]; int tj[5]; float txx[5];
-#pragma unroll
-            for (int q = 0; q < 5; q++) { tv[q] = -INFINITY; tj[q] = 0x7fffffff; txx[q] = 0.f; }
-            if (tid < 256) {
-                int tot = Kcur * NTLOG * 5;
-                for (int c = tid; c < tot; c += 256) {
-                    int k = c / (NTLOG * 5);
-                    if (t != 0 && sm.tk.end[k] != 0.f) continue;
-                    int rm = c - k * NTLOG * 5;
-                    int tile = rm / 5, q = rm - tile * 5;
-                    int n = b * Kcur + k;
-                    int gi = P.t5j[((size_t)tile * 160 + n) * 5 + q];
-                    if (gi == 0x7fffffff) continue;
-                    float x = P.t5v[((size_t)tile * 160 + n) * 5 + q];
-                    float lp  = __fsub_rn(__fsub_rn(x, sm.tk.mxs[k]), sm.tk.lgv[k]);
-                    float val = __fdiv_rn(__fadd_rn(lp, sm.tk.sc[k]), sm.tk.den[k]);
-                    ins5p(tv, tj, txx, val, k * Vv + gi, x);
-                }
-            }
-            if (tid == 0 && t != 0) {
-                for (int k = 0; k < Kcur; k++)
-                    if (sm.tk.end[k] != 0.f) {
-                        float val = __fdiv_rn(sm.tk.sc[k], sm.tk.den[k]);
-                        ins5p(tv, tj, txx, val, k * Vv + SEPTOK, 0.f);
-                    }
-            }
-            if (tid < 256) {
-#pragma unroll
-                for (int q = 0; q < 5; q++) {
-                    sm.tk.mv[tid * 5 + q] = tv[q];
-                    sm.tk.mj[tid * 5 + q] = tj[q];
-                    sm.tk.mxp[tid * 5 + q] = txx[q];
-                }
-            }
-            __syncthreads();
-            for (int pass = 0; pass < Kb; pass++) {
-                if (tid < 256) {
-                    float bv = -INFINITY; int bj = 0x7fffffff; float bx = 0.f;
-#pragma unroll
-                    for (int q = 0; q < 5; q++) {
-                        float v = sm.tk.mv[tid * 5 + q]; int j = sm.tk.mj[tid * 5 + q];
-                        if (betterf(v, j, bv, bj)) { bv = v; bj = j; bx = sm.tk.mxp[tid * 5 + q]; }
-                    }
-                    sm.tk.rv[tid] = bv; sm.tk.rj[tid] = bj; sm.tk.rx[tid] = bx;
-                }
-                __syncthreads();
-                for (int off = 128; off; off >>= 1) {
-                    if (tid < off) {
-                        float ov = sm.tk.rv[tid + off]; int oj = sm.tk.rj[tid + off];
-                        if (betterf(ov, oj, sm.tk.rv[tid], sm.tk.rj[tid])) {
-                            sm.tk.rv[tid] = ov; sm.tk.rj[tid] = oj;
-                            sm.tk.rx[tid] = sm.tk.rx[tid + off];
-                        }
-                    }
-                    __syncthreads();
-                }
-                if (tid == 0) { sm.tk.selj[pass] = sm.tk.rj[0]; sm.tk.selx[pass] = sm.tk.rx[0]; }
-                __syncthreads();
-                if (tid < 256) {
-#pragma unroll
-                    for (int q = 0; q < 5; q++)
-                        if (sm.tk.mj[tid * 5 + q] == sm.tk.selj[pass]) {
-                            sm.tk.mv[tid * 5 + q] = -INFINITY;
-                            sm.tk.mj[tid * 5 + q] = 0x7fffffff;
-                        }
-                }
-                __syncthreads();
-            }
-            if (tid == 0) {
-                for (int q = 0; q < Kb; q++) {
-                    int jj = sm.tk.selj[q];
-                    int pk = jj / Vv, vv = jj - pk * Vv;
-                    float lp;
-                    if (t == 0 || sm.tk.end[pk] == 0.f)
-                        lp = __fsub_rn(__fsub_rn(sm.tk.selx[q], sm.tk.mxs[pk]), sm.tk.lgv[pk]);
-                    else
-                        lp = (vv == SEPTOK) ? 0.f : -1e9f;
-                    float cand = __fadd_rn(lp, sm.tk.sc[pk]);
-                    P.scores[b * Kb + q]   = cand;
-                    P.toks_cur[b * Kb + q] = vv;
-                    P.maps_cur[b * Kb + q] = (t == 0) ? 0 : pk;
-                    if (t == 0) {
-                        P.ended[b * Kb + q]   = 0.f;
-                        P.lengths[b * Kb + q] = 0.f;
-                    } else {
-                        P.ended[b * Kb + q]   = (vv == SEPTOK) ? 1.f : sm.tk.end[q];
-                        P.lengths[b * Kb + q] = sm.tk.len[q];
-                    }
-                    P.toks_all[(size_t)t * Bb * Kb + b * Kb + q] = vv;
-                    P.maps_all[(size_t)t * Bb * Kb + b * Kb + q] = (t == 0) ? 0 : pk;
-                }
-            }
-            __syncthreads();
-        }
-        grid.sync();
-    }
-
-    if (blockIdx.x == 0 && tid < Bb) {
-        int b = tid;
-        int best = 0; float bvv = P.scores[b * Kb];
-        for (int k = 1; k < Kb; k++) {
-            float v = P.scores[b * Kb + k];
-            if (v > bvv) { bvv = v; best = k; }
-        }
-        int cur = best;
-        for (int t = Tt - 1; t >= 0; t--) {
-            P.outTok[b * Tt + t] = P.toks_all[t * Bb * Kb + b * Kb + cur];
-            cur = P.maps_all[t * Bb * Kb + b * Kb + cur];
-        }
+                lp = (vv == SEPTOK) ? 0.f : -1e9f;
+            float cand = __fadd_rn(lp, sc[pk]);
+            P.scores[b * Kb + q]   = cand;
+            P.toks_cur[b * Kb + q] = vv;
+            P.maps_cur[b * Kb + q] = (t == 0) ? 0 : pk;
+            if (t == 0) {
+                P.ended[b * Kb + q]   = 0.f;
+                P.lengths[b * Kb + q] = 0.f;
+            } else {
+                P.ended[b * Kb + q]   = (vv == SEPTOK) ? 1.f : endd[q];
+                P.lengths[b * Kb + q] = len[q];
+            }
+            P.toks_all[(size_t)t * Bb * Kb + b * Kb + q] = vv;
+            P.maps_all[(size_t)t * Bb * Kb + b * Kb + q] = (t == 0) ? 0 : pk;
+        }
+    }
+}
+
+__global__ void back_k(Params P)
+{
+    int b = threadIdx.x;
+    if (b >= Bb) return;
+    int best = 0; float bvv = P.scores[b * Kb];
+    for (int k = 1; k < Kb; k++) {
+        float v = P.scores[b * Kb + k];
+        if (v > bvv) { bvv = v; best = k; }
+    }
+    int cur = best;
+    for (int t = Tt - 1; t >= 0; t--) {
+        P.outTok[b * Tt + t] = P.toks_all[t * Bb * Kb + b * Kb + cur];
+        cur = P.maps_all[t * Bb * Kb + b * Kb + cur];
     }
 }
 
@@ -611,255 +605,6 @@
                 out[(size_t)gr * ldO + gi] = v;
             }
         }
-    }
-}
-
-__global__ __launch_bounds__(256) void gather_k(int N, int Kcur,
-    const int* __restrict__ maps, const int* __restrict__ toks,
-    const float* __restrict__ h_beam, const float* __restrict__ E,
-    float* __restrict__ h_g, float* __restrict__ xbuf)
-{
-    int n = blockIdx.x;
-    if (n >= N) return;
-    int b = n / Kcur;
-    int tok = toks ? toks[n] : SEPTOK;
-    const float* er = E + (size_t)tok * Hdim;
-    if (maps) {
-        const float* hs = h_beam + (size_t)(b * Kb + maps[n]) * Hdim;
-        for (int j = threadIdx.x; j < Hdim; j += 256) {
-            h_g[(size_t)n * Hdim + j]  = hs[j];
-            xbuf[(size_t)n * 1536 + j] = er[j];
-        }
-    } else {
-        for (int j = threadIdx.x; j < Hdim; j += 256) {
-            h_g[(size_t)n * Hdim + j]  = 0.f;
-            xbuf[(size_t)n * 1536 + j] = er[j];
-        }
-    }
-}
-
-__global__ __launch_bounds__(256) void bcast_k(const float* __restrict__ h_tmp,
-                                               float* __restrict__ h_beam)
-{
-    int b = blockIdx.x;
-    for (int j = threadIdx.x; j < Hdim; j += 256) {
-        float v = h_tmp[(size_t)b * Hdim + j];
-        for (int k = 0; k < Kb; k++)
-            h_beam[(size_t)(b * Kb + k) * Hdim + j] = v;
-    }
-}
-
-__global__ __launch_bounds__(256) void attn2_k(int N, int Kcur,
-    const float* __restrict__ hUa, const float* __restrict__ srcWa,
-    const float* __restrict__ src, const float* __restrict__ va,
-    float* __restrict__ xbuf)
-{
-    __shared__ float hu[Hdim];
-    __shared__ float va_s[Hdim];
-    __shared__ float e_s[Ss];
-    __shared__ float a_s[Ss];
-    int n = blockIdx.x, tid = threadIdx.x;
-    if (n >= N) return;
-    int b = n / Kcur;
-    for (int j = tid; j < Hdim; j += 256) {
-        hu[j]   = hUa[(size_t)n * Hdim + j];
-        va_s[j] = va[j];
-    }
-    __syncthreads();
-    int wv = tid >> 6, ln = tid & 63;
-    for (int s = wv * 16; s < wv * 16 + 16; s++) {
-        const float* sw = srcWa + (size_t)(b * Ss + s) * Hdim;
-        double p = 0.0;
-        for (int j = ln; j < Hdim; j += 64) {
-            float tv = (float)tanh((double)__fadd_rn(sw[j], hu[j]));
-            p = ::fma((double)tv, (double)va_s[j], p);
-        }
-        for (int off = 32; off; off >>= 1) p += __shfl_down(p, off, 64);
-        if (ln == 0) e_s[s] = (float)p;
-    }
-    __syncthreads();
-    if (tid < 64) {
-        float v = e_s[tid], m = v;
-        for (int off = 32; off; off >>= 1) m = fmaxf(m, __shfl_xor(m, off, 64));
-        float p = (float)exp((double)__fsub_rn(v, m));
-        double sum = (double)p;
-        for (int off = 32; off; off >>= 1) sum += __shfl_xor(sum, off, 64);
-        a_s[tid] = __fdiv_rn(p, (float)sum);
-    }
-    __syncthreads();
-    for (int j = tid; j < Hdim; j += 256) {
-        double acc = 0.0;
-        for (int s = 0; s < Ss; s++)
-            acc = ::fma((double)a_s[s], (double)src[(size_t)(b * Ss + s) * Hdim + j], acc);
-        xbuf[(size_t)n * 1536 + 768 + j] = (float)acc;
-    }
-}
-
-__global__ __launch_bounds__(256) void gate_k(int N,
-    const float* __restrict__ gx, const float* __restrict__ gh,
-    const float* __restrict__ h_g, float* __restrict__ h_out)
-{
-    int idx = blockIdx.x * 256 + threadIdx.x;
-    if (idx >= N * Hdim) return;
-    int n = idx / Hdim, i = idx - n * Hdim;
-    const float* gxr = gx + (size_t)n * 2304;
-    const float* ghr = gh + (size_t)n * 2304;
-    float xr = gxr[i], xz = gxr[768 + i], xn = gxr[1536 + i];
-    float hr = ghr[i], hz = ghr[768 + i], hn = ghr[1536 + i];
-    float r  = (float)(1.0 / (1.0 + exp(-(double)__fadd_rn(xr, hr))));
-    float z  = (float)(1.0 / (1.0 + exp(-(double)__fadd_rn(xz, hz))));
-    float nn = (float)tanh((double)__fadd_rn(xn, __fmul_rn(r, hn)));
-    float hv = h_g[(size_t)n * Hdim + i];
-    float h2 = __fadd_rn(__fmul_rn(__fsub_rn(1.f, z), nn), __fmul_rn(z, hv));
-    h_out[(size_t)n * Hdim + i] = h2;
-}
-
-__global__ __launch_bounds__(256) void lse_k(int N,
-    const float* __restrict__ logits, float* __restrict__ mx, float* __restrict__ lgs)
-{
-    __shared__ float  redf[256];
-    __shared__ double redd[256];
-    int n = blockIdx.x, tid = threadIdx.x;
-    const float* lg = logits + (size_t)n * Vv;
-    float m = -INFINITY;
-    for (int v = tid; v < Vv; v += 256) m = fmaxf(m, lg[v]);
-    redf[tid] = m; __syncthreads();
-    for (int off = 128; off; off >>= 1) {
-        if (tid < off) redf[tid] = fmaxf(redf[tid], redf[tid + off]);
-        __syncthreads();
-    }
-    m = redf[0];
-    double s = 0.0;
-    for (int v = tid; v < Vv; v += 256) {
-        float ex = (float)exp((double)__fsub_rn(lg[v], m));
-        s += (double)ex;
-    }
-    redd[tid] = s; __syncthreads();
-    for (int off = 128; off; off >>= 1) {
-        if (tid < off) redd[tid] += redd[tid + off];
-        __syncthreads();
-    }
-    if (tid == 0) {
-        mx[n] = m;
-        float sf = (float)redd[0];
-        lgs[n] = (float)log((double)sf);
-    }
-}
-
-__global__ __launch_bounds__(256) void topk5_k(int t,
-    const float* __restrict__ logits, const float* __restrict__ mx, const float* __restrict__ lgs,
-    float* scores, float* ended, float* lengths,
-    int* toks_cur, int* maps_cur, int* toks_all, int* maps_all)
-{
-    __shared__ float sc_s[Kb], den_s[Kb], end_s[Kb], len_s[Kb], mx_s[Kb], lg_s[Kb];
-    __shared__ float mv[256 * 5];
-    __shared__ int   mj[256 * 5];
-    __shared__ float rv[256];
-    __shared__ int   rj[256];
-    __shared__ int   selj[Kb];
-    int b = blockIdx.x, tid = threadIdx.x;
-    int Kcur = (t == 0) ? 1 : Kb;
-    if (tid < Kb) {
-        if (t == 0) {
-            sc_s[tid] = 0.f; end_s[tid] = 0.f; len_s[tid] = 0.f; den_s[tid] = 1.f;
-            mx_s[tid] = mx[b]; lg_s[tid] = lgs[b];
-        } else {
-            float e0 = ended[b * Kb + tid];
-            float ln = __fadd_rn(lengths[b * Kb + tid], (e0 == 0.f) ? 1.f : 0.f);
-            sc_s[tid]  = scores[b * Kb + tid];
-            end_s[tid] = e0;
-            len_s[tid] = ln;
-            den_s[tid] = (tid < Kb - 1) ? (float)pow((double)ln, (double)0.7f) : 1.f;
-            mx_s[tid]  = mx[b * Kb + tid];
-            lg_s[tid]  = lgs[b * Kb + tid];
-        }
-    }
-    __syncthreads();
-    const float* lbase = logits + (size_t)b * Kcur * Vv;
-    float tv[5]; int tj[5];
-#pragma unroll
-    for (int q = 0; q < 5; q++) { tv[q] = -INFINITY; tj[q] = 0x7fffffff; }
-    for (int k = 0; k < Kcur; k++) {
-        if (end_s[k] == 0.f) {
-            float m = mx_s[k], l = lg_s[k], sck = sc_s[k], den = den_s[k];
-            const float* lg = lbase + (size_t)k * Vv;
-            for (int v = tid; v < Vv; v += 256) {
-                float lp  = __fsub_rn(__fsub_rn(lg[v], m), l);
-                float val = __fdiv_rn(__fadd_rn(lp, sck), den);
-                ins5(tv, tj, val, k * Vv + v);
-            }
-        } else if (tid == 0) {
-            float val = __fdiv_rn(sc_s[k], den_s[k]);
-            ins5(tv, tj, val, k * Vv + SEPTOK);
-        }
-    }
-#pragma unroll
-    for (int q = 0; q < 5; q++) { mv[tid * 5 + q] = tv[q]; mj[tid * 5 + q] = tj[q]; }
-    __syncthreads();
-    for (int pass = 0; pass < Kb; pass++) {
-        float bv = -INFINITY; int bj = 0x7fffffff;
-#pragma unroll
-        for (int q = 0; q < 5; q++) {
-            float v = mv[tid * 5 + q]; int j = mj[tid * 5 + q];
-            if (betterf(v, j, bv, bj)) { bv = v; bj = j; }
-        }
-        rv[tid] = bv; rj[tid] = bj;
-        __syncthreads();
-        for (int off = 128; off; off >>= 1) {
-            if (tid < off) {
-                float ov = rv[tid + off]; int oj = rj[tid + off];
-                if (betterf(ov, oj, rv[tid], rj[tid])) { rv[tid] = ov; rj[tid] = oj; }
-            }
-            __syncthreads();
-        }
-        if (tid == 0) selj[pass] = rj[0];
-        __syncthreads();
-#pragma unroll
-        for (int q = 0; q < 5; q++)
-            if (mj[tid * 5 + q] == selj[pass]) { mv[tid * 5 + q] = -INFINITY; mj[tid * 5 + q] = 0x7fffffff; }
-        __syncthreads();
-    }
-    if (tid == 0) {
-        for (int q = 0; q < Kb; q++) {
-            int jj = selj[q];
-            int pk = jj / Vv, vv = jj - pk * Vv;
-            float lp;
-            if (end_s[pk] == 0.f)
-                lp = __fsub_rn(__fsub_rn(lbase[(size_t)pk * Vv + vv], mx_s[pk]), lg_s[pk]);
-            else
-                lp = (vv == SEPTOK) ? 0.f : -1e9f;
-            float cand = __fadd_rn(lp, sc_s[pk]);
-            scores[b * Kb + q]   = cand;
-            toks_cur[b * Kb + q] = vv;
-            maps_cur[b * Kb + q] = (t == 0) ? 0 : pk;
-            if (t == 0) {
-                ended[b * Kb + q]   = 0.f;
-                lengths[b * Kb + q] = 0.f;
-            } else {
-                ended[b * Kb + q]   = (vv == SEPTOK) ? 1.f : end_s[q];
-                lengths[b * Kb + q] = len_s[q];
-            }
-            toks_all[(size_t)t * Bb * Kb + b * Kb + q] = vv;
-            maps_all[(size_t)t * Bb * Kb + b * Kb + q] = (t == 0) ? 0 : pk;
-        }
-    }
-}
-
-__global__ void back_k(const float* __restrict__ scores,
-                       const int* __restrict__ toks_all, const int* __restrict__ maps_all,
-                       int* __restrict__ out)
-{
-    int b = threadIdx.x;
-    if (b >= Bb) return;
-    int best = 0; float bvv = scores[b * Kb];
-    for (int k = 1; k < Kb; k++) {
-        float v = scores[b * Kb + k];
-        if (v > bvv) { bvv = v; best = k; }
-    }
-    int cur = best;
-    for (int t = Tt - 1; t >= 0; t--) {
-        out[b * Tt + t] = toks_all[t * Bb * Kb + b * Kb + cur];
-        cur = maps_all[t * Bb * Kb + b * Kb + cur];
     }
 }
 
@@ -891,20 +636,13 @@
     P.srcWa   = (float*)alloc((size_t)Bb * Ss * Hdim * 4);
     P.hA      = (float*)alloc((size_t)Bb * Kb * Hdim * 4);
     P.hB      = (float*)alloc((size_t)Bb * Kb * Hdim * 4);
-    P.h_tmp   = (float*)alloc((size_t)Bb * Hdim * 4);
-    P.h_g     = (float*)alloc((size_t)Bb * Kb * Hdim * 4);
     P.hUa     = (float*)alloc((size_t)Bb * Kb * Hdim * 4);
-    P.xbuf    = (float*)alloc((size_t)Bb * Kb * 1536 * 4);
     P.gxE     = (float*)alloc((size_t)Bb * Kb * 2304 * 4);
-    P.gx      = (float*)alloc((size_t)Bb * Kb * 2304 * 4);
     P.gh      = (float*)alloc((size_t)Bb * Kb * 2304 * 4);
-    P.logits  = (float*)alloc((size_t)Bb * Kb * Vv * 4);
     P.mt_g    = (float*)alloc((size_t)NTLOG * 160 * 4);
     P.st_g    = (double*)alloc((size_t)NTLOG * 160 * 8);
     P.t5v     = (float*)alloc((size_t)NTLOG * 160 * 5 * 4);
     P.t5j     = (int*)alloc((size_t)NTLOG * 160 * 5 * 4);
-    P.mx      = (float*)alloc(Bb * Kb * 4);
-    P.lgs     = (float*)alloc(Bb * Kb * 4);
     P.scores  = (float*)alloc(Bb * Kb * 4);
     P.ended   = (float*)alloc(Bb * Kb * 4);
     P.lengths = (float*)alloc(Bb * Kb * 4);
@@ -916,67 +654,12 @@
     gemmN_k<8, 2, true><<<dim3(12, 16), 512, 0, stream>>>(
         Hdim, Hdim, Hdim, Hdim, P.src, P.Wa, nullptr, P.srcWa, Hdim);
 
-    int dev = 0;
-    (void)hipGetDevice(&dev);
-    int nCU = 256;
-    (void)hipDeviceGetAttribute(&nCU, hipDeviceAttributeMultiprocessorCount, dev);
-    int maxAct = 0;
-    if (hipOccupancyMaxActiveBlocksPerMultiprocessor(&maxAct, step_k, 512, 0)
-            != hipSuccess || maxAct < 1)
-        maxAct = 1;
-    long long gridLL = (long long)maxAct * (long long)nCU;
-    if (gridLL > 512) gridLL = 512;
-    if (gridLL < 1) gridLL = 1;
-    dim3 grid((unsigned)gridLL);
-
-    void* args[] = { (void*)&P };
-    hipError_t err = hipLaunchCooperativeKernel((void*)step_k, grid, dim3(512),
-                                                args, 0, stream);
-    if (err != hipSuccess) {
-        (void)hipGetLastError();
-        for (int t = 0; t < Tt; t++) {
-            int N  = (t == 0) ? Bb : Bb * Kb;
-            int Kc = (t == 0) ? 1 : Kb;
-            const int* mp = (t == 0) ? nullptr : P.maps_cur;
-            const int* tk = (t == 0) ? nullptr : P.toks_cur;
-            float* h_beam = P.hA;
-            float* h_cur = (t == 0) ? P.h_tmp : h_beam;
-
-            gather_k<<<N, 256, 0, stream>>>(N, Kc, mp, tk, h_beam, P.E, P.h_g, P.xbuf);
-            if (t == 0) {
-                gemmN_k<2, 2, true><<<dim3(12, 1), 512, 0, stream>>>(
-                    Hdim, Hdim, Hdim, Hdim, P.h_g, P.Ua, nullptr, P.hUa, Hdim);
-            } else {
-                gemmN_k<10, 2, true><<<dim3(12, 1), 512, 0, stream>>>(
-                    Hdim, Hdim, Hdim, Hdim, P.h_g, P.Ua, nullptr, P.hUa, Hdim);
-            }
-            attn2_k<<<N, 256, 0, stream>>>(N, Kc, P.hUa, P.srcWa, P.src, P.va, P.xbuf);
-            if (t == 0) {
-                gemmN_k<2, 2, false><<<dim3(36, 1), 512, 0, stream>>>(
-                    1536, 2304, 1536, 1536, P.xbuf, P.W_ih, P.b_ih, P.gx, 2304);
-                gemmN_k<2, 2, false><<<dim3(36, 1), 512, 0, stream>>>(
-                    Hdim, 2304, Hdim, Hdim, P.h_g, P.W_hh, P.b_hh, P.gh, 2304);
-            } else {
-                gemmN_k<10, 2, false><<<dim3(36, 1), 512, 0, stream>>>(
-                    1536, 2304, 1536, 1536, P.xbuf, P.W_ih, P.b_ih, P.gx, 2304);
-                gemmN_k<10, 2, false><<<dim3(36, 1), 512, 0, stream>>>(
-                    Hdim, 2304, Hdim, Hdim, P.h_g, P.W_hh, P.b_hh, P.gh, 2304);
-            }
-            gate_k<<<(N * Hdim + 255) / 256, 256, 0, stream>>>(N, P.gx, P.gh, P.h_g, h_cur);
-            if (t == 0)
-                bcast_k<<<Bb, 256, 0, stream>>>(P.h_tmp, h_beam);
-            if (t == 0) {
-                gemmN_k<2, 4, false><<<dim3(239, 1), 512, 0, stream>>>(
-                    Hdim, Vv, Hdim, Hdim, h_cur, P.Wo, P.bo, P.logits, Vv);
-            } else {
-                gemmN_k<10, 4, false><<<dim3(239, 1), 512, 0, stream>>>(
-                    Hdim, Vv, Hdim, Hdim, h_cur, P.Wo, P.bo, P.logits, Vv);
-            }
-            lse_k<<<N, 256, 0, stream>>>(N, P.logits, P.mx, P.lgs);
-            topk5_k<<<Bb, 256, 0, stream>>>(t, P.logits, P.mx, P.lgs, P.scores,
-                                            P.ended, P.lengths, P.toks_cur, P.maps_cur,
-                                            P.toks_all, P.maps_all);
-        }
-        back_k<<<1, 64, 0, stream>>>(P.scores, P.toks_all, P.maps_all, P.outTok);
-    }
-}
+    for (int t = 0; t < Tt; t++) {
+        int N = (t == 0) ? Bb : Bb * Kb;
+        p1_k<<<84, 512, 0, stream>>>(P, t, N);
+        p2_k<<<N, 512, 0, stream>>>(P, t, N);
+        p4_k<<<NTLOG, 512, 0, stream>>>(P, t, N);
+        p5_k<<<Bb, 512, 0, stream>>>(P, t);
+    }
+    back_k<<<1, 64, 0, stream>>>(P);
+}
```

After: 52.22 ms. 1.1x slower.
